# Kernel optimization log

Measured on AMD Instinct MI355X. Metric: run time of the kernel, lower is better.

## Reference

```python
import jax, jax.numpy as jnp
import numpy as np

B, S, V, D, H, DK, DFF, L = 2, 1024, 513, 512, 8, 64, 2048, 6
PAD_IDX = -1.0
EPS_GPE = 0.1

def _sinusoid_table(n_position, d_hid):
    pos = np.arange(n_position)[:, None].astype(np.float64)
    i = np.arange(d_hid)[None, :]
    angle = pos / np.power(10000.0, 2 * (i // 2) / d_hid)
    tab = np.zeros((n_position, d_hid), dtype=np.float32)
    tab[:, 0::2] = np.sin(angle[:, 0::2])
    tab[:, 1::2] = np.cos(angle[:, 1::2])
    return jnp.asarray(tab)

_POS_TABLE = _sinusoid_table(2048, D)

def _ln(x, g, b, eps=1e-6):
    m = x.mean(-1, keepdims=True)
    v = x.var(-1, keepdims=True)
    return (x - m) * jax.lax.rsqrt(v + eps) * g + b

def _mha(x_q, x_kv, wq_, wk_, wv_, wo_, mask, g, b):
    Bq, Sq, _ = x_q.shape
    Skv = x_kv.shape[1]
    q = (x_q @ wq_).reshape(Bq, Sq, H, DK).transpose(0, 2, 1, 3)
    k = (x_kv @ wk_).reshape(Bq, Skv, H, DK).transpose(0, 2, 1, 3)
    v = (x_kv @ wv_).reshape(Bq, Skv, H, DK).transpose(0, 2, 1, 3)
    scores = jnp.einsum('bhqd,bhkd->bhqk', q, k) / np.float32(np.sqrt(DK))
    scores = jnp.where(mask[:, None], scores, jnp.float32(-1e9))
    attn = jax.nn.softmax(scores, axis=-1)
    out = jnp.einsum('bhqk,bhkd->bhqd', attn, v).transpose(0, 2, 1, 3).reshape(Bq, Sq, D)
    return _ln(x_q + out @ wo_, g, b)

def _forward(dec_in, prev_dec_out, trg, adj, graph_length, gr_mask, gr_pos_enc_kernel,
             emb_w1, emb_b1, emb_w2, emb_b2, emb_w3, emb_b3, ln0_g, ln0_b,
             wq, wk, wv, wo, ln1_g, ln1_b,
             cq, ck, cv, co, ln2_g, ln2_b,
             ffn_w1, ffn_b1, ffn_w2, ffn_b2, ln3_g, ln3_b,
             p_w1, p_b1, p_w2, p_b2, p_w3, p_b3):
    # masks (n_ensemble = 1 so dec_in[:, :, 0, :] == dec_in)
    causal = jnp.tril(jnp.ones((S, S), bool))
    slf_mask = jnp.all(dec_in != PAD_IDX, -1)[:, None, :] & causal          # [B,S,S]
    enc_mask = jnp.all(prev_dec_out != PAD_IDX, -1)[:, None, :]             # [B,1,S]
    # word-embedding MLP: 513 -> 513 -> 513 -> 512
    h = jax.nn.relu(dec_in @ emb_w1 + emb_b1)
    h = jax.nn.relu(h @ emb_w2 + emb_b2)
    h = h @ emb_w3 + emb_b3                                                 # [B,S,D]
    # propagation graph positional encoding (k = 0..2, un-normalized branch)
    w = (1.0 - EPS_GPE) ** jnp.arange(gr_pos_enc_kernel.shape[1], dtype=jnp.float32)
    base = _POS_TABLE[:S]                                                   # [S,D]
    emb = jnp.einsum('k,bkst,td->bsd', w, gr_pos_enc_kernel, base) / w.sum()
    h = _ln(h + emb, ln0_g, ln0_b)
    for i in range(L):
        h = _mha(h, h, wq[i], wk[i], wv[i], wo[i], slf_mask, ln1_g[i], ln1_b[i])
        h = _mha(h, prev_dec_out, cq[i], ck[i], cv[i], co[i], enc_mask, ln2_g[i], ln2_b[i])
        f = jax.nn.relu(h @ ffn_w1[i] + ffn_b1[i]) @ ffn_w2[i] + ffn_b2[i]
        h = _ln(h + f, ln3_g[i], ln3_b[i])
    # projection head: 512 -> 513 -> 513 -> 513
    z = jax.nn.relu(h @ p_w1 + p_b1)
    z = jax.nn.relu(z @ p_w2 + p_b2)
    return z @ p_w3 + p_b3                                                  # [B,S,V]

def setup_inputs():
    key = jax.random.key(0)
    ks = jax.random.split(key, 24)
    def xavier(k, shape):
        lim = np.float32(np.sqrt(6.0 / (shape[-2] + shape[-1])))
        return jax.random.uniform(k, shape, jnp.float32, -lim, lim)
    inp = {}
    inp['dec_in'] = jax.random.uniform(ks[0], (B, S, V), jnp.float32)
    inp['prev_dec_out'] = jax.random.normal(ks[1], (B, S, D), jnp.float32)
    inp['trg'] = jnp.zeros((B, S, V), jnp.float32)
    inp['adj'] = jnp.zeros((B, S, S), jnp.float32)
    inp['graph_length'] = jnp.zeros((B, S, 10), jnp.float32)
    inp['gr_mask'] = jnp.zeros((B, 1, S, S), jnp.float32)
    gk = jax.random.uniform(ks[2], (B, 3, S, S), jnp.float32)
    inp['gr_pos_enc_kernel'] = gk / jnp.sum(gk, -1, keepdims=True)  # row-stochastic diffusion kernels
    SZ = max(V, D)  # sz_intermed = 513
    inp['emb_w1'] = xavier(ks[3], (V, SZ)); inp['emb_b1'] = jnp.zeros((SZ,))
    inp['emb_w2'] = xavier(ks[4], (SZ, SZ)); inp['emb_b2'] = jnp.zeros((SZ,))
    inp['emb_w3'] = xavier(ks[5], (SZ, D)); inp['emb_b3'] = jnp.zeros((D,))
    inp['ln0_g'] = jnp.ones((D,)); inp['ln0_b'] = jnp.zeros((D,))
    for name, ki, shp in [('wq', 6, (L, D, D)), ('wk', 7, (L, D, D)), ('wv', 8, (L, D, D)), ('wo', 9, (L, D, D)),
                          ('cq', 10, (L, D, D)), ('ck', 11, (L, D, D)), ('cv', 12, (L, D, D)), ('co', 13, (L, D, D)),
                          ('ffn_w1', 14, (L, D, DFF)), ('ffn_w2', 15, (L, DFF, D))]:
        inp[name] = xavier(ks[ki], shp)
    inp['ffn_b1'] = jnp.zeros((L, DFF)); inp['ffn_b2'] = jnp.zeros((L, D))
    inp['ln1_g'] = jnp.ones((L, D)); inp['ln1_b'] = jnp.zeros((L, D))
    inp['ln2_g'] = jnp.ones((L, D)); inp['ln2_b'] = jnp.zeros((L, D))
    inp['ln3_g'] = jnp.ones((L, D)); inp['ln3_b'] = jnp.zeros((L, D))
    inp['p_w1'] = xavier(ks[16], (D, V)); inp['p_b1'] = jnp.zeros((V,))
    inp['p_w2'] = xavier(ks[17], (V, V)); inp['p_b2'] = jnp.zeros((V,))
    inp['p_w3'] = xavier(ks[18], (V, V)); inp['p_b3'] = jnp.zeros((V,))
    return inp

def reference(dec_in, prev_dec_out, trg, adj, graph_length, gr_mask, gr_pos_enc_kernel,
              emb_w1, emb_b1, emb_w2, emb_b2, emb_w3, emb_b3, ln0_g, ln0_b,
              wq, wk, wv, wo, ln1_g, ln1_b,
              cq, ck, cv, co, ln2_g, ln2_b,
              ffn_w1, ffn_b1, ffn_w2, ffn_b2, ln3_g, ln3_b,
              p_w1, p_b1, p_w2, p_b2, p_w3, p_b3):
    return _forward(dec_in, prev_dec_out, trg, adj, graph_length, gr_mask, gr_pos_enc_kernel,
                    emb_w1, emb_b1, emb_w2, emb_b2, emb_w3, emb_b3, ln0_g, ln0_b,
                    wq, wk, wv, wo, ln1_g, ln1_b,
                    cq, ck, cv, co, ln2_g, ln2_b,
                    ffn_w1, ffn_b1, ffn_w2, ffn_b2, ln3_g, ln3_b,
                    p_w1, p_b1, p_w2, p_b2, p_w3, p_b3)
```

## Files before the change

kernel.cpp:

```cpp
#include <hip/hip_runtime.h>
#include <hip/hip_bf16.h>
#include <stdint.h>

#define BB 2
#define SS 1024
#define VV 513
#define VP 576
#define DD 512
#define HH 8
#define DKK 64
#define DFFN 2048
#define LL 6
#define MM (BB * SS)

typedef __bf16 bf16x8 __attribute__((ext_vector_type(8)));
typedef float f32x4 __attribute__((ext_vector_type(4)));
typedef unsigned short us8 __attribute__((ext_vector_type(8)));
typedef unsigned short us4 __attribute__((ext_vector_type(4)));

static __device__ inline unsigned short f2bf(float f) {
  union { float f; unsigned u; } v; v.f = f;
  unsigned u = v.u;
  unsigned r = (u + 0x7FFFu + ((u >> 16) & 1u)) >> 16;
  return (unsigned short)r;
}

static __device__ inline bf16x8 ldfrag(const unsigned short* p) {
  us8 r = *(const us8*)p;
  return __builtin_bit_cast(bf16x8, r);
}

typedef __attribute__((address_space(3))) void lds_void;
typedef const __attribute__((address_space(1))) void glb_void;
static __device__ inline void gl_lds16(const void* g, void* l) {
  __builtin_amdgcn_global_load_lds((glb_void*)g, (lds_void*)l, 16, 0, 0);
}

static __device__ inline bf16x8 ldfrag_swz(const unsigned short* base, int row, int kloc) {
  const unsigned byte = (unsigned)(row * 128 + kloc * 2) ^ (unsigned)((row & 7) << 4);
  return ldfrag((const unsigned short*)((const char*)base + byte));
}

static __device__ inline int rot3(int x) { return (x == 2) ? 0 : x + 1; }

struct GemmP {
  const unsigned short* A;
  const unsigned short* B0; const unsigned short* B1; const unsigned short* B2;
  const float* bias;
  float* C;
  unsigned short* D0; unsigned short* D1; unsigned short* D2;
  int Kp, Np, ldc, Nreal, relu;
};

template<int NB, int NT, int TRV, int KS>
__global__ __launch_bounds__(256)
void gemm_tpl(GemmP p)
{
  constexpr int FN = NT / 32;
  __shared__ unsigned short Al[3][64 * 64];
  __shared__ unsigned short Bl[3][NT * 64];
  const int tid = threadIdx.x;
  const int l = tid & 63, w = tid >> 6;
  const int wm = w >> 1, wn = w & 1;
  const int lr = l & 15, lg = l >> 4;

  const int nbn = p.Np / NT;
  int sel = 0, bx = blockIdx.x;
  if (NB > 1) { sel = bx / nbn; bx -= sel * nbn; }
  const unsigned short* Bmat = p.B0;
  if (NB > 1 && sel == 1) Bmat = p.B1;
  if (NB > 2 && sel == 2) Bmat = p.B2;
  const int m0 = blockIdx.y << 6, n0 = bx * NT;
  const int kz = (KS > 1) ? blockIdx.z : 0;

  f32x4 acc[2][FN];
  const f32x4 zf = {0.f, 0.f, 0.f, 0.f};
#pragma unroll
  for (int i = 0; i < 2; ++i)
#pragma unroll
    for (int j = 0; j < FN; ++j) acc[i][j] = zf;

  const size_t Kp = (size_t)p.Kp;
  const unsigned short* Abase = p.A + (size_t)m0 * Kp;
  const unsigned short* Bbase = Bmat + (size_t)n0 * Kp;
  const int nt = (p.Kp >> 6) / KS;
  const int kb0 = kz * nt;

  auto stage = [&](int buf, int kt) {
    const int k0 = (kb0 + kt) << 6;
#pragma unroll
    for (int j = 0; j < 2; ++j) {
      const int ti = j * 256 + tid;
      const int row = ti >> 3;
      const int ch = (ti & 7) ^ (row & 7);
      gl_lds16(Abase + (size_t)row * Kp + k0 + ch * 8, &Al[buf][ti * 8]);
    }
#pragma unroll
    for (int j = 0; j < FN; ++j) {
      const int ti = j * 256 + tid;
      const int row = ti >> 3;
      const int ch = (ti & 7) ^ (row & 7);
      gl_lds16(Bbase + (size_t)row * Kp + k0 + ch * 8, &Bl[buf][ti * 8]);
    }
  };

  stage(0, 0);
  if (nt > 1) stage(1, 1);
  int cb = 0, sb = 2;

  for (int kt = 0; kt < nt; ++kt) {
    if (kt + 1 < nt) {
      if constexpr (FN == 2) asm volatile("s_waitcnt vmcnt(4)" ::: "memory");
      else                   asm volatile("s_waitcnt vmcnt(6)" ::: "memory");
    } else {
      asm volatile("s_waitcnt vmcnt(0)" ::: "memory");
    }
    __builtin_amdgcn_s_barrier();
    if (kt + 2 < nt) { stage(sb, kt + 2); sb = rot3(sb); }
#pragma unroll
    for (int ks = 0; ks < 2; ++ks) {
      bf16x8 af[2], bfv[FN];
#pragma unroll
      for (int mf = 0; mf < 2; ++mf)
        af[mf] = ldfrag_swz(Al[cb], wm * 32 + mf * 16 + lr, ks * 32 + lg * 8);
#pragma unroll
      for (int nf = 0; nf < FN; ++nf)
        bfv[nf] = ldfrag_swz(Bl[cb], wn * (NT / 2) + nf * 16 + lr, ks * 32 + lg * 8);
#pragma unroll
      for (int mf = 0; mf < 2; ++mf)
#pragma unroll
        for (int nf = 0; nf < FN; ++nf)
          acc[mf][nf] = __builtin_amdgcn_mfma_f32_16x16x32_bf16(af[mf], bfv[nf], acc[mf][nf], 0, 0, 0);
    }
    cb = rot3(cb);
  }

  unsigned short* Dsel = p.D0;
  if (NB > 1 && sel == 1) Dsel = p.D1;
  if (NB > 2 && sel == 2) Dsel = p.D2;

  if (TRV && sel == 2) {
#pragma unroll
    for (int mf = 0; mf < 2; ++mf) {
      const int growb = m0 + wm * 32 + mf * 16 + (lg << 2);
      const int b = growb >> 10, s = growb & 1023;
#pragma unroll
      for (int nf = 0; nf < FN; ++nf) {
        const int gcol = n0 + wn * (NT / 2) + nf * 16 + lr;
        const int h = gcol >> 6, d = gcol & 63;
        us4 t;
#pragma unroll
        for (int r = 0; r < 4; ++r) t[r] = f2bf(acc[mf][nf][r]);
        *(us4*)(Dsel + (((size_t)(b * HH) + h) * DKK + d) * SS + s) = t;
      }
    }
    return;
  }

  float* Cz = p.C ? (p.C + (size_t)kz * MM * p.ldc) : nullptr;
#pragma unroll
  for (int mf = 0; mf < 2; ++mf) {
#pragma unroll
    for (int r = 0; r < 4; ++r) {
      const int grow = m0 + wm * 32 + mf * 16 + (lg << 2) + r;
#pragma unroll
      for (int nf = 0; nf < FN; ++nf) {
        const int gcol = n0 + wn * (NT / 2) + nf * 16 + lr;
        float v = acc[mf][nf][r];
        if (p.bias && kz == 0 && gcol < p.Nreal) v += p.bias[gcol];
        if (p.relu) v = fmaxf(v, 0.f);
        if (Dsel) Dsel[(size_t)grow * p.Np + gcol] = f2bf(v);
        if (Cz && gcol < p.Nreal) Cz[(size_t)grow * p.ldc + gcol] = v;
      }
    }
  }
}

struct GemmBat {
  const unsigned short* A;
  const unsigned short* B[12];
  unsigned short* D[12];
  int Kp, Np;
};

__global__ __launch_bounds__(256)
void gemm_bat(GemmBat p)
{
  __shared__ unsigned short Al[3][64 * 64];
  __shared__ unsigned short Bl[3][64 * 64];
  const int tid = threadIdx.x;
  const int l = tid & 63, w = tid >> 6;
  const int wm = w >> 1, wn = w & 1;
  const int lr = l & 15, lg = l >> 4;

  const int nbn = p.Np >> 6;
  const int sel = blockIdx.x / nbn;
  const int bx = blockIdx.x - sel * nbn;
  const unsigned short* Bmat = p.B[sel];
  unsigned short* Dmat = p.D[sel];
  const int m0 = blockIdx.y << 6, n0 = bx << 6;

  f32x4 acc[2][2];
  const f32x4 zf = {0.f, 0.f, 0.f, 0.f};
#pragma unroll
  for (int i = 0; i < 2; ++i)
#pragma unroll
    for (int j = 0; j < 2; ++j) acc[i][j] = zf;

  const size_t Kp = (size_t)p.Kp;
  const unsigned short* Abase = p.A + (size_t)m0 * Kp;
  const unsigned short* Bbase = Bmat + (size_t)n0 * Kp;

  auto stage = [&](int buf, int kt) {
    const int k0 = kt << 6;
#pragma unroll
    for (int j = 0; j < 2; ++j) {
      const int ti = j * 256 + tid;
      const int row = ti >> 3;
      const int ch = (ti & 7) ^ (row & 7);
      gl_lds16(Abase + (size_t)row * Kp + k0 + ch * 8, &Al[buf][ti * 8]);
    }
#pragma unroll
    for (int j = 0; j < 2; ++j) {
      const int ti = j * 256 + tid;
      const int row = ti >> 3;
      const int ch = (ti & 7) ^ (row & 7);
      gl_lds16(Bbase + (size_t)row * Kp + k0 + ch * 8, &Bl[buf][ti * 8]);
    }
  };

  const int nt = p.Kp >> 6;
  stage(0, 0);
  if (nt > 1) stage(1, 1);
  int cb = 0, sb = 2;

  for (int kt = 0; kt < nt; ++kt) {
    if (kt + 1 < nt) asm volatile("s_waitcnt vmcnt(4)" ::: "memory");
    else             asm volatile("s_waitcnt vmcnt(0)" ::: "memory");
    __builtin_amdgcn_s_barrier();
    if (kt + 2 < nt) { stage(sb, kt + 2); sb = rot3(sb); }
#pragma unroll
    for (int ks = 0; ks < 2; ++ks) {
      bf16x8 af[2], bfv[2];
#pragma unroll
      for (int mf = 0; mf < 2; ++mf)
        af[mf] = ldfrag_swz(Al[cb], wm * 32 + mf * 16 + lr, ks * 32 + lg * 8);
#pragma unroll
      for (int nf = 0; nf < 2; ++nf)
        bfv[nf] = ldfrag_swz(Bl[cb], wn * 32 + nf * 16 + lr, ks * 32 + lg * 8);
#pragma unroll
      for (int mf = 0; mf < 2; ++mf)
#pragma unroll
        for (int nf = 0; nf < 2; ++nf)
          acc[mf][nf] = __builtin_amdgcn_mfma_f32_16x16x32_bf16(af[mf], bfv[nf], acc[mf][nf], 0, 0, 0);
    }
    cb = rot3(cb);
  }

  if (sel & 1) {
#pragma unroll
    for (int mf = 0; mf < 2; ++mf) {
      const int growb = m0 + wm * 32 + mf * 16 + (lg << 2);
      const int b = growb >> 10, s = growb & 1023;
#pragma unroll
      for (int nf = 0; nf < 2; ++nf) {
        const int gcol = n0 + wn * 32 + nf * 16 + lr;
        const int h = gcol >> 6, d = gcol & 63;
        us4 t;
#pragma unroll
        for (int r = 0; r < 4; ++r) t[r] = f2bf(acc[mf][nf][r]);
        *(us4*)(Dmat + (((size_t)(b * HH) + h) * DKK + d) * SS + s) = t;
      }
    }
    return;
  }

#pragma unroll
  for (int mf = 0; mf < 2; ++mf) {
#pragma unroll
    for (int r = 0; r < 4; ++r) {
      const int grow = m0 + wm * 32 + mf * 16 + (lg << 2) + r;
#pragma unroll
      for (int nf = 0; nf < 2; ++nf) {
        const int gcol = n0 + wn * 32 + nf * 16 + lr;
        Dmat[(size_t)grow * p.Np + gcol] = f2bf(acc[mf][nf][r]);
      }
    }
  }
}

__global__ __launch_bounds__(128)
void attn_kernel(const unsigned short* __restrict__ Qb,
                 const unsigned short* __restrict__ Kb,
                 const unsigned short* __restrict__ VbT,
                 unsigned short* __restrict__ Ob,
                 const float* __restrict__ maskadd)
{
  __shared__ unsigned short Kl[2][2][64 * 64];
  __shared__ unsigned short Vl[2][2][64 * 64];
  __shared__ char PC[9216];
  unsigned short* Pl = (unsigned short*)PC;
  float (*comb)[66] = (float(*)[66])PC;

  const int tid = threadIdx.x;
  const int l = tid & 63, w = tid >> 6;
  const int qt = blockIdx.x, h = blockIdx.y, b = blockIdx.z;
  const int lr = l & 15, lg = l >> 4;

  bf16x8 qf[2][2];
#pragma unroll
  for (int mf = 0; mf < 2; ++mf) {
    const unsigned short* qrow = Qb + ((size_t)(b * SS) + qt * 32 + mf * 16 + lr) * DD + h * DKK;
    qf[mf][0] = ldfrag(qrow + (lg << 3));
    qf[mf][1] = ldfrag(qrow + 32 + (lg << 3));
  }

  const unsigned short* Kbase = Kb + (size_t)(b * SS) * DD + h * DKK;
  const unsigned short* Vbase = VbT + ((size_t)(b * HH) + h) * DKK * SS;

  auto stage = [&](int buf, int kt) {
#pragma unroll
    for (int j = 0; j < 8; ++j) {
      const int ti = j * 64 + l;
      const int row = ti >> 3;
      const int ch = (ti & 7) ^ (row & 7);
      gl_lds16(Kbase + (size_t)(kt * 64 + row) * DD + ch * 8, &Kl[w][buf][ti * 8]);
    }
#pragma unroll
    for (int j = 0; j < 8; ++j) {
      const int ti = j * 64 + l;
      const int row = ti >> 3;
      const int ch = (ti & 7) ^ (row & 7);
      gl_lds16(Vbase + (size_t)row * SS + kt * 64 + ch * 8, &Vl[w][buf][ti * 8]);
    }
  };

  f32x4 accO[2][4];
  const f32x4 zf = {0.f, 0.f, 0.f, 0.f};
#pragma unroll
  for (int mf = 0; mf < 2; ++mf)
#pragma unroll
    for (int nf = 0; nf < 4; ++nf) accO[mf][nf] = zf;
  float mold[2][4], lsum[2][4];
#pragma unroll
  for (int mf = 0; mf < 2; ++mf)
#pragma unroll
    for (int r = 0; r < 4; ++r) { mold[mf][r] = -1e30f; lsum[mf][r] = 0.f; }

  const int ktmax = (qt >> 1) + 1;
  const int myn = (ktmax - w + 1) >> 1;

  if (myn > 0) stage(0, w);
  int buf = 0;

  for (int i = 0; i < myn; ++i) {
    const int kt = w + 2 * i;
    if (i + 1 < myn) {
      stage(buf ^ 1, kt + 2);
      asm volatile("s_waitcnt vmcnt(16)" ::: "memory");
    } else {
      asm volatile("s_waitcnt vmcnt(0)" ::: "memory");
    }
    const unsigned short* KB = &Kl[w][buf][0];
    const unsigned short* VB = &Vl[w][buf][0];
    float sc[2][4][4];
    __builtin_amdgcn_s_setprio(1);
#pragma unroll
    for (int nf = 0; nf < 4; ++nf) {
      bf16x8 k0 = ldfrag_swz(KB, nf * 16 + lr, lg * 8);
      bf16x8 k1 = ldfrag_swz(KB, nf * 16 + lr, 32 + lg * 8);
      const int kglob = kt * 64 + nf * 16 + lr;
      const float madd = maskadd[b * SS + kglob];
#pragma unroll
      for (int mf = 0; mf < 2; ++mf) {
        f32x4 s = zf;
        s = __builtin_amdgcn_mfma_f32_16x16x32_bf16(qf[mf][0], k0, s, 0, 0, 0);
        s = __builtin_amdgcn_mfma_f32_16x16x32_bf16(qf[mf][1], k1, s, 0, 0, 0);
#pragma unroll
        for (int r = 0; r < 4; ++r) {
          const int qglob = qt * 32 + mf * 16 + (lg << 2) + r;
          sc[mf][nf][r] = (kglob > qglob) ? -1e9f : s[r] * 0.125f + madd;
        }
      }
    }
    __builtin_amdgcn_s_setprio(0);
#pragma unroll
    for (int mf = 0; mf < 2; ++mf)
#pragma unroll
      for (int r = 0; r < 4; ++r) {
        float mloc = fmaxf(fmaxf(sc[mf][0][r], sc[mf][1][r]), fmaxf(sc[mf][2][r], sc[mf][3][r]));
#pragma unroll
        for (int off = 1; off < 16; off <<= 1)
          mloc = fmaxf(mloc, __shfl_xor(mloc, off, 64));
        const float mnew = fmaxf(mold[mf][r], mloc);
        const float corr = __expf(mold[mf][r] - mnew);
        float ps = 0.f;
#pragma unroll
        for (int nf = 0; nf < 4; ++nf) {
          const float pv = __expf(sc[mf][nf][r] - mnew);
          sc[mf][nf][r] = pv;
          ps += pv;
        }
#pragma unroll
        for (int off = 1; off < 16; off <<= 1)
          ps += __shfl_xor(ps, off, 64);
        lsum[mf][r] = lsum[mf][r] * corr + ps;
#pragma unroll
        for (int nf = 0; nf < 4; ++nf) accO[mf][nf][r] *= corr;
        mold[mf][r] = mnew;
      }
    unsigned short* pw = Pl + w * 32 * 72;
#pragma unroll
    for (int mf = 0; mf < 2; ++mf)
#pragma unroll
      for (int nf = 0; nf < 4; ++nf)
#pragma unroll
        for (int r = 0; r < 4; ++r)
          pw[(mf * 16 + (lg << 2) + r) * 72 + nf * 16 + lr] = f2bf(sc[mf][nf][r]);
    bf16x8 pa[2][2];
#pragma unroll
    for (int mf = 0; mf < 2; ++mf) {
      pa[mf][0] = ldfrag(&pw[(mf * 16 + lr) * 72 + (lg << 3)]);
      pa[mf][1] = ldfrag(&pw[(mf * 16 + lr) * 72 + 32 + (lg << 3)]);
    }
    __builtin_amdgcn_s_setprio(1);
#pragma unroll
    for (int nf = 0; nf < 4; ++nf) {
      bf16x8 v0 = ldfrag_swz(VB, nf * 16 + lr, lg * 8);
      bf16x8 v1 = ldfrag_swz(VB, nf * 16 + lr, 32 + lg * 8);
#pragma unroll
      for (int mf = 0; mf < 2; ++mf) {
        accO[mf][nf] = __builtin_amdgcn_mfma_f32_16x16x32_bf16(pa[mf][0], v0, accO[mf][nf], 0, 0, 0);
        accO[mf][nf] = __builtin_amdgcn_mfma_f32_16x16x32_bf16(pa[mf][1], v1, accO[mf][nf], 0, 0, 0);
      }
    }
    __builtin_amdgcn_s_setprio(0);
    buf ^= 1;
  }

  __syncthreads();
  if (w == 1) {
#pragma unroll
    for (int mf = 0; mf < 2; ++mf)
#pragma unroll
      for (int r = 0; r < 4; ++r) {
        const int qrow = mf * 16 + (lg << 2) + r;
#pragma unroll
        for (int nf = 0; nf < 4; ++nf)
          comb[qrow][nf * 16 + lr] = accO[mf][nf][r];
        if (lr == 0) { comb[qrow][64] = mold[mf][r]; comb[qrow][65] = lsum[mf][r]; }
      }
  }
  __syncthreads();
  if (w == 0) {
#pragma unroll
    for (int mf = 0; mf < 2; ++mf)
#pragma unroll
      for (int r = 0; r < 4; ++r) {
        const int qrow = mf * 16 + (lg << 2) + r;
        const float m1 = comb[qrow][64], l1 = comb[qrow][65];
        const float m0v = mold[mf][r], l0 = lsum[mf][r];
        const float ms = fmaxf(m0v, m1);
        const float f0 = __expf(m0v - ms), f1 = __expf(m1 - ms);
        const float inv = 1.f / (l0 * f0 + l1 * f1);
        const size_t orow = ((size_t)(b * SS) + qt * 32 + mf * 16 + (lg << 2) + r) * DD + h * DKK;
#pragma unroll
        for (int nf = 0; nf < 4; ++nf)
          Ob[orow + nf * 16 + lr] =
              f2bf((accO[mf][nf][r] * f0 + comb[qrow][nf * 16 + lr] * f1) * inv);
      }
  }
}

__global__ __launch_bounds__(128)
void attnx_kernel(const unsigned short* __restrict__ Hb,
                  const unsigned short* __restrict__ Wq,
                  const unsigned short* __restrict__ Kb,
                  const unsigned short* __restrict__ VbT,
                  unsigned short* __restrict__ Ob,
                  const float* __restrict__ maskadd)
{
  __shared__ unsigned short Kl[2][2][64 * 64];
  __shared__ unsigned short Vl[2][2][64 * 64];
  __shared__ char PC[9216];
  unsigned short* Pl = (unsigned short*)PC;
  float (*comb)[66] = (float(*)[66])PC;
  unsigned short* QA = &Kl[0][0][0];
  unsigned short* QB = &Vl[0][0][0];
  unsigned short* Ql = (unsigned short*)PC;

  const int tid = threadIdx.x;
  const int l = tid & 63, w = tid >> 6;
  const int qt = blockIdx.x, h = blockIdx.y, b = blockIdx.z;
  const int lr = l & 15, lg = l >> 4;

  {
    const unsigned short* Abase = Hb + ((size_t)(b * SS) + qt * 32) * DD;
    const unsigned short* Bbase = Wq + (size_t)(h * DKK) * DD;
    auto stage_q = [&](int buf, int kt) {
      const int k0 = kt << 6;
#pragma unroll
      for (int j = 0; j < 2; ++j) {
        const int ti = j * 128 + tid;
        const int row = ti >> 3;
        const int ch = (ti & 7) ^ (row & 7);
        gl_lds16(Abase + (size_t)row * DD + k0 + ch * 8, &QA[buf * 2048 + ti * 8]);
      }
#pragma unroll
      for (int j = 0; j < 4; ++j) {
        const int ti = j * 128 + tid;
        const int row = ti >> 3;
        const int ch = (ti & 7) ^ (row & 7);
        gl_lds16(Bbase + (size_t)row * DD + k0 + ch * 8, &QB[buf * 4096 + ti * 8]);
      }
    };
    f32x4 qacc[2][2];
    const f32x4 zf = {0.f, 0.f, 0.f, 0.f};
#pragma unroll
    for (int i = 0; i < 2; ++i)
#pragma unroll
      for (int j = 0; j < 2; ++j) qacc[i][j] = zf;

    stage_q(0, 0);
    for (int kt = 0; kt < 8; ++kt) {
      if (kt + 1 < 8) {
        stage_q((kt + 1) & 1, kt + 1);
        asm volatile("s_waitcnt vmcnt(6)" ::: "memory");
      } else {
        asm volatile("s_waitcnt vmcnt(0)" ::: "memory");
      }
      __builtin_amdgcn_s_barrier();
      const unsigned short* qa = &QA[(kt & 1) * 2048];
      const unsigned short* qbuf = &QB[(kt & 1) * 4096];
#pragma unroll
      for (int ks = 0; ks < 2; ++ks) {
        bf16x8 af[2], bfv[2];
#pragma unroll
        for (int mf = 0; mf < 2; ++mf)
          af[mf] = ldfrag_swz(qa, mf * 16 + lr, ks * 32 + lg * 8);
#pragma unroll
        for (int nf = 0; nf < 2; ++nf)
          bfv[nf] = ldfrag_swz(qbuf, w * 32 + nf * 16 + lr, ks * 32 + lg * 8);
#pragma unroll
        for (int mf = 0; mf < 2; ++mf)
#pragma unroll
          for (int nf = 0; nf < 2; ++nf)
            qacc[mf][nf] = __builtin_amdgcn_mfma_f32_16x16x32_bf16(af[mf], bfv[nf], qacc[mf][nf], 0, 0, 0);
      }
      __builtin_amdgcn_s_barrier();
    }
#pragma unroll
    for (int mf = 0; mf < 2; ++mf)
#pragma unroll
      for (int nf = 0; nf < 2; ++nf)
#pragma unroll
        for (int r = 0; r < 4; ++r)
          Ql[(mf * 16 + (lg << 2) + r) * 72 + w * 32 + nf * 16 + lr] = f2bf(qacc[mf][nf][r] * 0.125f);
    __syncthreads();
  }
  bf16x8 qf[2][2];
#pragma unroll
  for (int mf = 0; mf < 2; ++mf) {
    qf[mf][0] = ldfrag(&Ql[(mf * 16 + lr) * 72 + (lg << 3)]);
    qf[mf][1] = ldfrag(&Ql[(mf * 16 + lr) * 72 + 32 + (lg << 3)]);
  }
  __syncthreads();

  const unsigned short* Kbase = Kb + (size_t)(b * SS) * DD + h * DKK;
  const unsigned short* Vbase = VbT + ((size_t)(b * HH) + h) * DKK * SS;

  auto stage = [&](int buf, int kt) {
#pragma unroll
    for (int j = 0; j < 8; ++j) {
      const int ti = j * 64 + l;
      const int row = ti >> 3;
      const int ch = (ti & 7) ^ (row & 7);
      gl_lds16(Kbase + (size_t)(kt * 64 + row) * DD + ch * 8, &Kl[w][buf][ti * 8]);
    }
#pragma unroll
    for (int j = 0; j < 8; ++j) {
      const int ti = j * 64 + l;
      const int row = ti >> 3;
      const int ch = (ti & 7) ^ (row & 7);
      gl_lds16(Vbase + (size_t)row * SS + kt * 64 + ch * 8, &Vl[w][buf][ti * 8]);
    }
  };

  f32x4 accO[2][4];
  const f32x4 zf = {0.f, 0.f, 0.f, 0.f};
#pragma unroll
  for (int mf = 0; mf < 2; ++mf)
#pragma unroll
    for (int nf = 0; nf < 4; ++nf) accO[mf][nf] = zf;
  float mold[2][4], lsum[2][4];
#pragma unroll
  for (int mf = 0; mf < 2; ++mf)
#pragma unroll
    for (int r = 0; r < 4; ++r) { mold[mf][r] = -1e30f; lsum[mf][r] = 0.f; }

  const int myn = (SS / 64 - w + 1) >> 1;
  stage(0, w);
  int buf = 0;

  for (int i = 0; i < myn; ++i) {
    const int kt = w + 2 * i;
    if (i + 1 < myn) {
      stage(buf ^ 1, kt + 2);
      asm volatile("s_waitcnt vmcnt(16)" ::: "memory");
    } else {
      asm volatile("s_waitcnt vmcnt(0)" ::: "memory");
    }
    const unsigned short* KB = &Kl[w][buf][0];
    const unsigned short* VB = &Vl[w][buf][0];
    float sc[2][4][4];
    __builtin_amdgcn_s_setprio(1);
#pragma unroll
    for (int nf = 0; nf < 4; ++nf) {
      bf16x8 k0 = ldfrag_swz(KB, nf * 16 + lr, lg * 8);
      bf16x8 k1 = ldfrag_swz(KB, nf * 16 + lr, 32 + lg * 8);
      const int kglob = kt * 64 + nf * 16 + lr;
      const float madd = maskadd[b * SS + kglob];
#pragma unroll
      for (int mf = 0; mf < 2; ++mf) {
        f32x4 s = zf;
        s = __builtin_amdgcn_mfma_f32_16x16x32_bf16(qf[mf][0], k0, s, 0, 0, 0);
        s = __builtin_amdgcn_mfma_f32_16x16x32_bf16(qf[mf][1], k1, s, 0, 0, 0);
#pragma unroll
        for (int r = 0; r < 4; ++r)
          sc[mf][nf][r] = s[r] + madd;
      }
    }
    __builtin_amdgcn_s_setprio(0);
#pragma unroll
    for (int mf = 0; mf < 2; ++mf)
#pragma unroll
      for (int r = 0; r < 4; ++r) {
        float mloc = fmaxf(fmaxf(sc[mf][0][r], sc[mf][1][r]), fmaxf(sc[mf][2][r], sc[mf][3][r]));
#pragma unroll
        for (int off = 1; off < 16; off <<= 1)
          mloc = fmaxf(mloc, __shfl_xor(mloc, off, 64));
        const float mnew = fmaxf(mold[mf][r], mloc);
        const float corr = __expf(mold[mf][r] - mnew);
        float ps = 0.f;
#pragma unroll
        for (int nf = 0; nf < 4; ++nf) {
          const float pv = __expf(sc[mf][nf][r] - mnew);
          sc[mf][nf][r] = pv;
          ps += pv;
        }
#pragma unroll
        for (int off = 1; off < 16; off <<= 1)
          ps += __shfl_xor(ps, off, 64);
        lsum[mf][r] = lsum[mf][r] * corr + ps;
#pragma unroll
        for (int nf = 0; nf < 4; ++nf) accO[mf][nf][r] *= corr;
        mold[mf][r] = mnew;
      }
    unsigned short* pw = Pl + w * 32 * 72;
#pragma unroll
    for (int mf = 0; mf < 2; ++mf)
#pragma unroll
      for (int nf = 0; nf < 4; ++nf)
#pragma unroll
        for (int r = 0; r < 4; ++r)
          pw[(mf * 16 + (lg << 2) + r) * 72 + nf * 16 + lr] = f2bf(sc[mf][nf][r]);
    bf16x8 pa[2][2];
#pragma unroll
    for (int mf = 0; mf < 2; ++mf) {
      pa[mf][0] = ldfrag(&pw[(mf * 16 + lr) * 72 + (lg << 3)]);
      pa[mf][1] = ldfrag(&pw[(mf * 16 + lr) * 72 + 32 + (lg << 3)]);
    }
    __builtin_amdgcn_s_setprio(1);
#pragma unroll
    for (int nf = 0; nf < 4; ++nf) {
      bf16x8 v0 = ldfrag_swz(VB, nf * 16 + lr, lg * 8);
      bf16x8 v1 = ldfrag_swz(VB, nf * 16 + lr, 32 + lg * 8);
#pragma unroll
      for (int mf = 0; mf < 2; ++mf) {
        accO[mf][nf] = __builtin_amdgcn_mfma_f32_16x16x32_bf16(pa[mf][0], v0, accO[mf][nf], 0, 0, 0);
        accO[mf][nf] = __builtin_amdgcn_mfma_f32_16x16x32_bf16(pa[mf][1], v1, accO[mf][nf], 0, 0, 0);
      }
    }
    __builtin_amdgcn_s_setprio(0);
    buf ^= 1;
  }

  __syncthreads();
  if (w == 1) {
#pragma unroll
    for (int mf = 0; mf < 2; ++mf)
#pragma unroll
      for (int r = 0; r < 4; ++r) {
        const int qrow = mf * 16 + (lg << 2) + r;
#pragma unroll
        for (int nf = 0; nf < 4; ++nf)
          comb[qrow][nf * 16 + lr] = accO[mf][nf][r];
        if (lr == 0) { comb[qrow][64] = mold[mf][r]; comb[qrow][65] = lsum[mf][r]; }
      }
  }
  __syncthreads();
  if (w == 0) {
#pragma unroll
    for (int mf = 0; mf < 2; ++mf)
#pragma unroll
      for (int r = 0; r < 4; ++r) {
        const int qrow = mf * 16 + (lg << 2) + r;
        const float m1 = comb[qrow][64], l1 = comb[qrow][65];
        const float m0v = mold[mf][r], l0 = lsum[mf][r];
        const float ms = fmaxf(m0v, m1);
        const float f0 = __expf(m0v - ms), f1 = __expf(m1 - ms);
        const float inv = 1.f / (l0 * f0 + l1 * f1);
        const size_t orow = ((size_t)(b * SS) + qt * 32 + mf * 16 + (lg << 2) + r) * DD + h * DKK;
#pragma unroll
        for (int nf = 0; nf < 4; ++nf)
          Ob[orow + nf * 16 + lr] =
              f2bf((accO[mf][nf][r] * f0 + comb[qrow][nf * 16 + lr] * f1) * inv);
      }
  }
}

template<int P>
__global__ __launch_bounds__(256)
void addln_kernel(const float* __restrict__ a, const float* __restrict__ c,
                  const float* __restrict__ g, const float* __restrict__ bb,
                  float* __restrict__ hf, unsigned short* __restrict__ hb)
{
  const int row = blockIdx.x * 4 + (threadIdx.x >> 6);
  const int l = threadIdx.x & 63;
  const float* ar = a + (size_t)row * DD + l * 8;
  f32x4 x0 = *(const f32x4*)ar;
  f32x4 x1 = *(const f32x4*)(ar + 4);
#pragma unroll
  for (int pp = 0; pp < P; ++pp) {
    const float* cr = c + (size_t)pp * MM * DD + (size_t)row * DD + l * 8;
    x0 += *(const f32x4*)cr;
    x1 += *(const f32x4*)(cr + 4);
  }
  float sum = x0[0] + x0[1] + x0[2] + x0[3] + x1[0] + x1[1] + x1[2] + x1[3];
#pragma unroll
  for (int off = 1; off < 64; off <<= 1) sum += __shfl_xor(sum, off, 64);
  const float mean = sum * (1.f / 512.f);
  float vs = 0.f;
#pragma unroll
  for (int j = 0; j < 4; ++j) { float d0 = x0[j] - mean; float d1 = x1[j] - mean; vs += d0 * d0 + d1 * d1; }
#pragma unroll
  for (int off = 1; off < 64; off <<= 1) vs += __shfl_xor(vs, off, 64);
  const float rs = rsqrtf(vs * (1.f / 512.f) + 1e-6f);
  const f32x4 g0 = *(const f32x4*)(g + l * 8), g1 = *(const f32x4*)(g + l * 8 + 4);
  const f32x4 b0 = *(const f32x4*)(bb + l * 8), b1 = *(const f32x4*)(bb + l * 8 + 4);
  f32x4 o0, o1;
  us8 ob;
#pragma unroll
  for (int j = 0; j < 4; ++j) {
    o0[j] = (x0[j] - mean) * rs * g0[j] + b0[j];
    o1[j] = (x1[j] - mean) * rs * g1[j] + b1[j];
    ob[j] = f2bf(o0[j]); ob[j + 4] = f2bf(o1[j]);
  }
  float* of = hf + (size_t)row * DD + l * 8;
  *(f32x4*)of = o0; *(f32x4*)(of + 4) = o1;
  *(us8*)(hb + (size_t)row * DD + l * 8) = ob;
}

__global__ __launch_bounds__(256)
void prep_all(const float* __restrict__ dec_in, const float* __restrict__ prev,
              unsigned short* __restrict__ decb, unsigned short* __restrict__ prevb,
              float* __restrict__ kvs, float* __restrict__ kve,
              unsigned short* __restrict__ tabT,
              const float* __restrict__ gk, unsigned short* __restrict__ Mb)
{
  const int blk = blockIdx.x, tid = threadIdx.x;
  if (blk < 1024) {
    const int isdec = blk < 512;
    const int row = (isdec ? blk : blk - 512) * 4 + (tid >> 6);
    const int l = tid & 63;
    const int NC = isdec ? VV : DD, NP = isdec ? VP : DD;
    const float* xr = (isdec ? dec_in : prev) + (size_t)row * NC;
    unsigned short* ob = (isdec ? decb : prevb) + (size_t)row * NP;
    int ok = 1;
    for (int j = l; j < NP; j += 64) {
      if (j < NC) {
        const float v = xr[j];
        ok &= (v != -1.0f) ? 1 : 0;
        ob[j] = f2bf(v);
      } else ob[j] = 0;
    }
    ok = __all(ok) ? 1 : 0;
    if (l == 0) (isdec ? kvs : kve)[row] = ok ? 0.f : -1e9f;
  } else if (blk < 3072) {
    const int i = (blk - 1024) * 256 + tid;
    const int d = i >> 10, s = i & 1023;
    const float ex = (float)(2 * (d >> 1)) * (1.0f / (float)DD);
    const float ang = (float)s * exp2f(ex * -13.287712379549449f);
    tabT[i] = f2bf((d & 1) ? cosf(ang) : sinf(ang));
  } else {
    const int i = (blk - 3072) * 256 + tid;
    const int b = i / (SS * SS);
    const int rem = i - b * (SS * SS);
    const float* p = gk + (size_t)b * 3 * SS * SS + rem;
    Mb[i] = f2bf((p[0] + 0.9f * p[SS * SS] + 0.81f * p[2 * SS * SS]) * (1.0f / 2.71f));
  }
}

struct WJobs {
  const float* W[8]; unsigned short* WT[8];
  int K[8], N[8], Kp[8], Np[8], nbx[8], nby[8];
  int off[9];
};
__global__ __launch_bounds__(256)
void wconv_all(WJobs p)
{
  __shared__ float t[64][65];
  const int bid = blockIdx.x;
  int j = 0;
#pragma unroll
  for (int i = 0; i < 8; ++i) if (bid >= p.off[i + 1]) j = i + 1;
  const int local = bid - p.off[j];
  const int per = p.nbx[j] * p.nby[j];
  const int z = local / per;
  const int rem = local - z * per;
  const int by = rem / p.nbx[j];
  const int bx = rem - by * p.nbx[j];
  const int K = p.K[j], N = p.N[j], Kp = p.Kp[j], Np = p.Np[j];
  const float* Wl = p.W[j] + (size_t)z * K * N;
  unsigned short* WTl = p.WT[j] + (size_t)z * Np * Kp;
  const int n0 = bx << 6, k0 = by << 6;
  const int cx = threadIdx.x & 63, ry = threadIdx.x >> 6;
#pragma unroll
  for (int i = 0; i < 16; ++i) {
    const int kk = k0 + ry + i * 4, nn = n0 + cx;
    t[ry + i * 4][cx] = (kk < K && nn < N) ? Wl[(size_t)kk * N + nn] : 0.f;
  }
  __syncthreads();
#pragma unroll
  for (int i = 0; i < 16; ++i) {
    const int nn = n0 + ry + i * 4, kk = k0 + cx;
    if (nn < Np && kk < Kp) WTl[(size_t)nn * Kp + kk] = f2bf(t[cx][ry + i * 4]);
  }
}

struct WconvB { const float* W[8]; unsigned short* WT[8]; };
__global__ __launch_bounds__(256)
void wconv8_kernel(WconvB p)
{
  __shared__ float t[64][65];
  const int z = blockIdx.z;
  const int wi = z / LL, li = z - wi * LL;
  const float* Wl = p.W[wi] + (size_t)li * DD * DD;
  unsigned short* WTl = p.WT[wi] + (size_t)li * DD * DD;
  const int n0 = blockIdx.x << 6, k0 = blockIdx.y << 6;
  const int cx = threadIdx.x & 63, ry = threadIdx.x >> 6;
#pragma unroll
  for (int i = 0; i < 16; ++i)
    t[ry + i * 4][cx] = Wl[(size_t)(k0 + ry + i * 4) * DD + n0 + cx];
  __syncthreads();
#pragma unroll
  for (int i = 0; i < 16; ++i)
    WTl[(size_t)(n0 + ry + i * 4) * DD + k0 + cx] = f2bf(t[cx][ry + i * 4]);
}

static inline void g1(hipStream_t s, const unsigned short* A, const unsigned short* B,
                      const float* bias, float* C, unsigned short* D,
                      int Kp, int Np, int ldc, int Nreal, int relu)
{
  GemmP p{};
  p.A = A; p.B0 = B; p.bias = bias; p.C = C; p.D0 = D;
  p.Kp = Kp; p.Np = Np; p.ldc = ldc; p.Nreal = Nreal; p.relu = relu;
  gemm_tpl<1, 64, 0, 1><<<dim3(Np >> 6, MM >> 6), 256, 0, s>>>(p);
}

static inline void g1w(hipStream_t s, const unsigned short* A, const unsigned short* B,
                       const float* bias, unsigned short* D, int Kp, int Np, int relu)
{
  GemmP p{};
  p.A = A; p.B0 = B; p.bias = bias; p.D0 = D;
  p.Kp = Kp; p.Np = Np; p.ldc = Np; p.Nreal = Np; p.relu = relu;
  gemm_tpl<1, 128, 0, 1><<<dim3(Np >> 7, MM >> 6), 256, 0, s>>>(p);
}

template<int KS>
static inline void g1k(hipStream_t s, const unsigned short* A, const unsigned short* B,
                       const float* bias, float* C, int Kp)
{
  GemmP p{};
  p.A = A; p.B0 = B; p.bias = bias; p.C = C;
  p.Kp = Kp; p.Np = DD; p.ldc = DD; p.Nreal = DD; p.relu = 0;
  gemm_tpl<1, 64, 0, KS><<<dim3(DD >> 6, MM >> 6, KS), 256, 0, s>>>(p);
}

static inline void g3t(hipStream_t s, const unsigned short* A, const unsigned short* B0,
                       const unsigned short* B1, const unsigned short* B2,
                       unsigned short* D0, unsigned short* D1, unsigned short* D2T)
{
  GemmP p{};
  p.A = A; p.B0 = B0; p.B1 = B1; p.B2 = B2; p.D0 = D0; p.D1 = D1; p.D2 = D2T;
  p.Kp = DD; p.Np = DD; p.ldc = DD; p.Nreal = DD; p.relu = 0;
  gemm_tpl<3, 64, 1, 1><<<dim3(3 * (DD >> 6), MM >> 6), 256, 0, s>>>(p);
}

extern "C" void kernel_launch(void* const* d_in, const int* in_sizes, int n_in,
                              void* d_out, int out_size, void* d_ws, size_t ws_size,
                              hipStream_t stream)
{
  (void)in_sizes; (void)n_in; (void)out_size; (void)ws_size;
  const float* dec_in = (const float*)d_in[0];
  const float* prev   = (const float*)d_in[1];
  const float* gk     = (const float*)d_in[6];
  const float* emb_w1 = (const float*)d_in[7];
  const float* emb_b1 = (const float*)d_in[8];
  const float* emb_w2 = (const float*)d_in[9];
  const float* emb_b2 = (const float*)d_in[10];
  const float* emb_w3 = (const float*)d_in[11];
  const float* emb_b3 = (const float*)d_in[12];
  const float* ln0_g  = (const float*)d_in[13];
  const float* ln0_b  = (const float*)d_in[14];
  const float* wq     = (const float*)d_in[15];
  const float* wk     = (const float*)d_in[16];
  const float* wv     = (const float*)d_in[17];
  const float* wo     = (const float*)d_in[18];
  const float* cq     = (const float*)d_in[19];
  const float* ck     = (const float*)d_in[20];
  const float* cv     = (const float*)d_in[21];
  const float* co     = (const float*)d_in[22];
  const float* ffn_w1 = (const float*)d_in[23];
  const float* ffn_w2 = (const float*)d_in[24];
  const float* ffn_b1 = (const float*)d_in[25];
  const float* ffn_b2 = (const float*)d_in[26];
  const float* ln1_g  = (const float*)d_in[27];
  const float* ln1_b  = (const float*)d_in[28];
  const float* ln2_g  = (const float*)d_in[29];
  const float* ln2_b  = (const float*)d_in[30];
  const float* ln3_g  = (const float*)d_in[31];
  const float* ln3_b  = (const float*)d_in[32];
  const float* p_w1   = (const float*)d_in[33];
  const float* p_b1   = (const float*)d_in[34];
  const float* p_w2   = (const float*)d_in[35];
  const float* p_b2   = (const float*)d_in[36];
  const float* p_w3   = (const float*)d_in[37];
  const float* p_b3   = (const float*)d_in[38];

  char* wsp = (char*)d_ws;
  auto carve = [&](size_t bytes) { char* r = wsp; wsp += (bytes + 255) & ~(size_t)255; return r; };

  unsigned short* decb  = (unsigned short*)carve((size_t)MM * VP * 2);
  unsigned short* prevb = (unsigned short*)carve((size_t)MM * DD * 2);
  float*          hf    = (float*)carve((size_t)MM * DD * 4);
  unsigned short* hb    = (unsigned short*)carve((size_t)MM * DD * 2);
  float*          xf1   = (float*)carve((size_t)MM * DD * 4);
  unsigned short* tb1   = (unsigned short*)carve((size_t)MM * DFFN * 2);
  unsigned short* Mbb   = tb1;
  float*          xf2   = (float*)((char*)tb1 + (size_t)MM * SS * 2);
  unsigned short* tb2a  = (unsigned short*)carve((size_t)MM * VP * 2);
  unsigned short* tb2b  = (unsigned short*)carve((size_t)MM * VP * 2);
  unsigned short* qb    = (unsigned short*)carve((size_t)MM * DD * 2);
  unsigned short* kb    = (unsigned short*)carve((size_t)MM * DD * 2);
  unsigned short* vbT   = (unsigned short*)carve((size_t)MM * DD * 2);
  float* kvs = (float*)carve((size_t)MM * 4);
  float* kve = (float*)carve((size_t)MM * 4);
  unsigned short* postabt = (unsigned short*)carve((size_t)DD * SS * 2);
  unsigned short* ew1t  = (unsigned short*)carve((size_t)VP * VP * 2);
  unsigned short* ew2t  = (unsigned short*)carve((size_t)VP * VP * 2);
  unsigned short* ew3t  = (unsigned short*)carve((size_t)DD * VP * 2);
  unsigned short* wqt   = (unsigned short*)carve((size_t)LL * DD * DD * 2);
  unsigned short* wkt   = (unsigned short*)carve((size_t)LL * DD * DD * 2);
  unsigned short* wvt   = (unsigned short*)carve((size_t)LL * DD * DD * 2);
  unsigned short* wot   = (unsigned short*)carve((size_t)LL * DD * DD * 2);
  unsigned short* cqt   = (unsigned short*)carve((size_t)LL * DD * DD * 2);
  unsigned short* ckt   = (unsigned short*)carve((size_t)LL * DD * DD * 2);
  unsigned short* cvt   = (unsigned short*)carve((size_t)LL * DD * DD * 2);
  unsigned short* cot   = (unsigned short*)carve((size_t)LL * DD * DD * 2);
  unsigned short* f1t   = (unsigned short*)carve((size_t)LL * DFFN * DD * 2);
  unsigned short* f2t   = (unsigned short*)carve((size_t)LL * DD * DFFN * 2);
  unsigned short* p1t   = (unsigned short*)carve((size_t)VP * DD * 2);
  unsigned short* p2t   = (unsigned short*)carve((size_t)VP * VP * 2);
  unsigned short* p3t   = (unsigned short*)carve((size_t)VP * VP * 2);
  unsigned short* ckall = (unsigned short*)carve((size_t)LL * MM * DD * 2);
  unsigned short* cvbT  = (unsigned short*)carve((size_t)LL * MM * DD * 2);
  float*          xk4   = (float*)carve((size_t)4 * MM * DD * 4);

  const dim3 agrid(SS / 32, HH, BB);

  prep_all<<<11264, 256, 0, stream>>>(dec_in, prev, decb, prevb, kvs, kve, postabt, gk, Mbb);

  {
    WconvB wb{};
    wb.W[0] = wq; wb.W[1] = wk; wb.W[2] = wv; wb.W[3] = wo;
    wb.W[4] = cq; wb.W[5] = ck; wb.W[6] = cv; wb.W[7] = co;
    wb.WT[0] = wqt; wb.WT[1] = wkt; wb.WT[2] = wvt; wb.WT[3] = wot;
    wb.WT[4] = cqt; wb.WT[5] = ckt; wb.WT[6] = cvt; wb.WT[7] = cot;
    wconv8_kernel<<<dim3(8, 8, 8 * LL), 256, 0, stream>>>(wb);
  }
  {
    WJobs wj{};
    const float* Ws[8]   = {emb_w1, emb_w2, emb_w3, ffn_w1, ffn_w2, p_w1, p_w2, p_w3};
    unsigned short* Ds[8] = {ew1t, ew2t, ew3t, f1t, f2t, p1t, p2t, p3t};
    const int Ks[8]  = {VV, VV, VV, DD, DFFN, DD, VV, VV};
    const int Ns[8]  = {VV, VV, DD, DFFN, DD, VV, VV, VV};
    const int Kps[8] = {VP, VP, VP, DD, DFFN, DD, VP, VP};
    const int Nps[8] = {VP, VP, DD, DFFN, DD, VP, VP, VP};
    const int nls[8] = {1, 1, 1, LL, LL, 1, 1, 1};
    int off = 0;
    for (int j = 0; j < 8; ++j) {
      wj.W[j] = Ws[j]; wj.WT[j] = Ds[j];
      wj.K[j] = Ks[j]; wj.N[j] = Ns[j]; wj.Kp[j] = Kps[j]; wj.Np[j] = Nps[j];
      wj.nbx[j] = (Nps[j] + 63) / 64; wj.nby[j] = (Kps[j] + 63) / 64;
      wj.off[j] = off;
      off += wj.nbx[j] * wj.nby[j] * nls[j];
    }
    wj.off[8] = off;
    wconv_all<<<off, 256, 0, stream>>>(wj);
  }

  {
    GemmBat p{};
    p.A = prevb; p.Kp = DD; p.Np = DD;
    for (int i = 0; i < LL; ++i) {
      p.B[2 * i]     = ckt + (size_t)i * DD * DD;
      p.B[2 * i + 1] = cvt + (size_t)i * DD * DD;
      p.D[2 * i]     = ckall + (size_t)i * MM * DD;
      p.D[2 * i + 1] = cvbT + (size_t)i * MM * DD;
    }
    gemm_bat<<<dim3(12 * (DD >> 6), MM >> 6), 256, 0, stream>>>(p);
  }

  g1(stream, decb, ew1t, emb_b1, nullptr, tb2a, VP, VP, VP, VV, 1);
  g1(stream, tb2a, ew2t, emb_b2, nullptr, tb2b, VP, VP, VP, VV, 1);
  g1(stream, tb2b, ew3t, emb_b3, xf1, nullptr, VP, DD, DD, DD, 0);
  g1(stream, Mbb, postabt, nullptr, xf2, nullptr, SS, DD, DD, DD, 0);
  addln_kernel<1><<<MM / 4, 256, 0, stream>>>(xf1, xf2, ln0_g, ln0_b, hf, hb);

  for (int i = 0; i < LL; ++i) {
    const size_t od = (size_t)i * DD * DD;
    g3t(stream, hb, wqt + od, wkt + od, wvt + od, qb, kb, vbT);
    attn_kernel<<<agrid, 128, 0, stream>>>(qb, kb, vbT, qb, kvs);
    g1k<2>(stream, qb, wot + od, nullptr, xk4, DD);
    addln_kernel<2><<<MM / 4, 256, 0, stream>>>(hf, xk4, ln1_g + i * DD, ln1_b + i * DD, hf, hb);
    attnx_kernel<<<agrid, 128, 0, stream>>>(hb, cqt + od, ckall + (size_t)i * MM * DD,
                                            cvbT + (size_t)i * MM * DD, qb, kve);
    g1k<2>(stream, qb, cot + od, nullptr, xk4, DD);
    addln_kernel<2><<<MM / 4, 256, 0, stream>>>(hf, xk4, ln2_g + i * DD, ln2_b + i * DD, hf, hb);
    g1w(stream, hb, f1t + (size_t)i * DFFN * DD, ffn_b1 + i * DFFN, tb1, DD, DFFN, 1);
    g1k<4>(stream, tb1, f2t + (size_t)i * DD * DFFN, ffn_b2 + i * DD, xk4, DFFN);
    addln_kernel<4><<<MM / 4, 256, 0, stream>>>(hf, xk4, ln3_g + i * DD, ln3_b + i * DD, hf, hb);
  }

  g1(stream, hb, p1t, p_b1, nullptr, tb2a, DD, VP, VP, VV, 1);
  g1(stream, tb2a, p2t, p_b2, nullptr, tb2b, VP, VP, VP, VV, 1);
  g1(stream, tb2b, p3t, p_b3, (float*)d_out, nullptr, VP, VP, VV, VV, 0);
}
```

Before: 994.0 us.

## Fuse FFN GEMMs and layernorm into one cooperative kernel; merge prologue launches

Replaces the per-layer FFN sequence (up-projection GEMM, split-K down-projection GEMM, add+layernorm) with a single cooperative kernel that runs persistent work loops separated by grid-wide syncs. It also merges the three prologue kernels (input prep and the two weight-conversion kernels) into one launch and switches the positional-encoding GEMM to split-K. The aim is to cut kernel launch overhead and tail gaps between dependent stages. The cost is grid.sync overhead, and the grid is capped at 512 blocks, which may leave parallelism unused in the GEMM phases.

```diff
diff --git a/kernel.cpp b/kernel.cpp
--- a/kernel.cpp
+++ b/kernel.cpp
@@ -1,6 +1,9 @@
 #include <hip/hip_runtime.h>
 #include <hip/hip_bf16.h>
+#include <hip/hip_cooperative_groups.h>
 #include <stdint.h>
+
+namespace cg = cooperative_groups;
 
 #define BB 2
 #define SS 1024
@@ -43,6 +46,171 @@
 
 static __device__ inline int rot3(int x) { return (x == 2) ? 0 : x + 1; }
 
+template<int NT>
+__device__ __forceinline__ void gemm_item(
+    unsigned short* Al, unsigned short* Bl,
+    const unsigned short* Abase, const unsigned short* Bbase,
+    int Kp, int nt, int kb0,
+    const float* bias, int applybias, int relu,
+    unsigned short* D, int ldD, int m0, int n0,
+    float* Cz, int ldc)
+{
+  constexpr int FN = NT / 32;
+  const int tid = threadIdx.x;
+  const int l = tid & 63, w = tid >> 6;
+  const int wm = w >> 1, wn = w & 1;
+  const int lr = l & 15, lg = l >> 4;
+
+  f32x4 acc[2][FN];
+  const f32x4 zf = {0.f, 0.f, 0.f, 0.f};
+#pragma unroll
+  for (int i = 0; i < 2; ++i)
+#pragma unroll
+    for (int j = 0; j < FN; ++j) acc[i][j] = zf;
+
+  auto stage = [&](int buf, int kt) {
+    const int k0 = (kb0 + kt) << 6;
+#pragma unroll
+    for (int j = 0; j < 2; ++j) {
+      const int ti = j * 256 + tid;
+      const int row = ti >> 3;
+      const int ch = (ti & 7) ^ (row & 7);
+      gl_lds16(Abase + (size_t)row * Kp + k0 + ch * 8, &Al[buf * 4096 + ti * 8]);
+    }
+#pragma unroll
+    for (int j = 0; j < FN; ++j) {
+      const int ti = j * 256 + tid;
+      const int row = ti >> 3;
+      const int ch = (ti & 7) ^ (row & 7);
+      gl_lds16(Bbase + (size_t)row * Kp + k0 + ch * 8, &Bl[buf * (NT * 64) + ti * 8]);
+    }
+  };
+
+  stage(0, 0);
+  if (nt > 1) stage(1, 1);
+  int cb = 0, sb = 2;
+
+  for (int kt = 0; kt < nt; ++kt) {
+    if (kt + 1 < nt) {
+      if constexpr (FN == 2) asm volatile("s_waitcnt vmcnt(4)" ::: "memory");
+      else                   asm volatile("s_waitcnt vmcnt(6)" ::: "memory");
+    } else {
+      asm volatile("s_waitcnt vmcnt(0)" ::: "memory");
+    }
+    __builtin_amdgcn_s_barrier();
+    if (kt + 2 < nt) { stage(sb, kt + 2); sb = rot3(sb); }
+#pragma unroll
+    for (int ks = 0; ks < 2; ++ks) {
+      bf16x8 af[2], bfv[FN];
+#pragma unroll
+      for (int mf = 0; mf < 2; ++mf)
+        af[mf] = ldfrag_swz(Al + cb * 4096, wm * 32 + mf * 16 + lr, ks * 32 + lg * 8);
+#pragma unroll
+      for (int nf = 0; nf < FN; ++nf)
+        bfv[nf] = ldfrag_swz(Bl + cb * (NT * 64), wn * (NT / 2) + nf * 16 + lr, ks * 32 + lg * 8);
+#pragma unroll
+      for (int mf = 0; mf < 2; ++mf)
+#pragma unroll
+        for (int nf = 0; nf < FN; ++nf)
+          acc[mf][nf] = __builtin_amdgcn_mfma_f32_16x16x32_bf16(af[mf], bfv[nf], acc[mf][nf], 0, 0, 0);
+    }
+    cb = rot3(cb);
+  }
+
+#pragma unroll
+  for (int mf = 0; mf < 2; ++mf) {
+#pragma unroll
+    for (int r = 0; r < 4; ++r) {
+      const int grow = m0 + wm * 32 + mf * 16 + (lg << 2) + r;
+#pragma unroll
+      for (int nf = 0; nf < FN; ++nf) {
+        const int gcol = n0 + wn * (NT / 2) + nf * 16 + lr;
+        float v = acc[mf][nf][r];
+        if (bias && applybias) v += bias[gcol];
+        if (relu) v = fmaxf(v, 0.f);
+        if (D) D[(size_t)grow * ldD + gcol] = f2bf(v);
+        if (Cz) Cz[(size_t)grow * ldc + gcol] = v;
+      }
+    }
+  }
+}
+
+template<int P>
+__device__ __forceinline__ void addln_item(int wi, const float* a, const float* c,
+    const float* g, const float* bb, float* hf, unsigned short* hb)
+{
+  const int row = wi * 4 + (threadIdx.x >> 6);
+  const int l = threadIdx.x & 63;
+  const float* ar = a + (size_t)row * DD + l * 8;
+  f32x4 x0 = *(const f32x4*)ar;
+  f32x4 x1 = *(const f32x4*)(ar + 4);
+#pragma unroll
+  for (int pp = 0; pp < P; ++pp) {
+    const float* cr = c + (size_t)pp * MM * DD + (size_t)row * DD + l * 8;
+    x0 += *(const f32x4*)cr;
+    x1 += *(const f32x4*)(cr + 4);
+  }
+  float sum = x0[0] + x0[1] + x0[2] + x0[3] + x1[0] + x1[1] + x1[2] + x1[3];
+#pragma unroll
+  for (int off = 1; off < 64; off <<= 1) sum += __shfl_xor(sum, off, 64);
+  const float mean = sum * (1.f / 512.f);
+  float vs = 0.f;
+#pragma unroll
+  for (int j = 0; j < 4; ++j) { float d0 = x0[j] - mean; float d1 = x1[j] - mean; vs += d0 * d0 + d1 * d1; }
+#pragma unroll
+  for (int off = 1; off < 64; off <<= 1) vs += __shfl_xor(vs, off, 64);
+  const float rs = rsqrtf(vs * (1.f / 512.f) + 1e-6f);
+  const f32x4 g0 = *(const f32x4*)(g + l * 8), g1 = *(const f32x4*)(g + l * 8 + 4);
+  const f32x4 b0 = *(const f32x4*)(bb + l * 8), b1 = *(const f32x4*)(bb + l * 8 + 4);
+  f32x4 o0, o1;
+  us8 ob;
+#pragma unroll
+  for (int j = 0; j < 4; ++j) {
+    o0[j] = (x0[j] - mean) * rs * g0[j] + b0[j];
+    o1[j] = (x1[j] - mean) * rs * g1[j] + b1[j];
+    ob[j] = f2bf(o0[j]); ob[j + 4] = f2bf(o1[j]);
+  }
+  float* of = hf + (size_t)row * DD + l * 8;
+  *(f32x4*)of = o0; *(f32x4*)(of + 4) = o1;
+  *(us8*)(hb + (size_t)row * DD + l * 8) = ob;
+}
+
+struct FfnP {
+  const unsigned short* hb;
+  const unsigned short* f1t; const float* b1;
+  unsigned short* tb1;
+  const unsigned short* f2t; const float* b2;
+  float* xk4;
+  const float* hf; const float* gamma; const float* beta;
+  float* hfout; unsigned short* hbout;
+};
+
+__global__ __launch_bounds__(256)
+void coop_ffn(FfnP p)
+{
+  __shared__ unsigned short Al[3 * 4096];
+  __shared__ unsigned short Bl[3 * 128 * 64];
+  cg::grid_group grid = cg::this_grid();
+
+  for (int wi = blockIdx.x; wi < 512; wi += gridDim.x) {
+    const int bx = wi & 15, by = wi >> 4;
+    gemm_item<128>(Al, Bl,
+                   p.hb + (size_t)(by * 64) * DD, p.f1t + (size_t)(bx * 128) * DD,
+                   DD, 8, 0, p.b1, 1, 1, p.tb1, DFFN, by * 64, bx * 128, nullptr, 0);
+  }
+  grid.sync();
+  for (int wi = blockIdx.x; wi < 1024; wi += gridDim.x) {
+    const int kz = wi >> 8, rem = wi & 255, by = rem >> 3, bx = rem & 7;
+    gemm_item<64>(Al, Bl,
+                  p.tb1 + (size_t)(by * 64) * DFFN, p.f2t + (size_t)(bx * 64) * DFFN,
+                  DFFN, 8, kz * 8, p.b2, kz == 0, 0, nullptr, 0, by * 64, bx * 64,
+                  p.xk4 + (size_t)kz * MM * DD, DD);
+  }
+  grid.sync();
+  for (int wi = blockIdx.x; wi < 512; wi += gridDim.x)
+    addln_item<4>(wi, p.hf, p.xk4, p.gamma, p.beta, p.hfout, p.hbout);
+}
+
 struct GemmP {
   const unsigned short* A;
   const unsigned short* B0; const unsigned short* B1; const unsigned short* B2;
@@ -57,8 +225,8 @@
 void gemm_tpl(GemmP p)
 {
   constexpr int FN = NT / 32;
-  __shared__ unsigned short Al[3][64 * 64];
-  __shared__ unsigned short Bl[3][NT * 64];
+  __shared__ unsigned short Al[3 * 4096];
+  __shared__ unsigned short Bl[3 * NT * 64];
   const int tid = threadIdx.x;
   const int l = tid & 63, w = tid >> 6;
   const int wm = w >> 1, wn = w & 1;
@@ -73,6 +241,16 @@
   const int m0 = blockIdx.y << 6, n0 = bx * NT;
   const int kz = (KS > 1) ? blockIdx.z : 0;
 
+  if (!(TRV && sel == 2)) {
+    unsigned short* Dsel = p.D0;
+    if (NB > 1 && sel == 1) Dsel = p.D1;
+    float* Cz = p.C ? (p.C + (size_t)kz * MM * p.ldc) : nullptr;
+    gemm_item<NT>(Al, Bl, p.A + (size_t)m0 * p.Kp, Bmat + (size_t)n0 * p.Kp,
+                  p.Kp, (p.Kp >> 6) / KS, kz * ((p.Kp >> 6) / KS),
+                  p.bias, kz == 0, p.relu, Dsel, p.Np, m0, n0, Cz, p.ldc);
+    return;
+  }
+
   f32x4 acc[2][FN];
   const f32x4 zf = {0.f, 0.f, 0.f, 0.f};
 #pragma unroll
@@ -83,38 +261,32 @@
   const size_t Kp = (size_t)p.Kp;
   const unsigned short* Abase = p.A + (size_t)m0 * Kp;
   const unsigned short* Bbase = Bmat + (size_t)n0 * Kp;
-  const int nt = (p.Kp >> 6) / KS;
-  const int kb0 = kz * nt;
+  const int nt = p.Kp >> 6;
 
   auto stage = [&](int buf, int kt) {
-    const int k0 = (kb0 + kt) << 6;
+    const int k0 = kt << 6;
 #pragma unroll
     for (int j = 0; j < 2; ++j) {
       const int ti = j * 256 + tid;
       const int row = ti >> 3;
       const int ch = (ti & 7) ^ (row & 7);
-      gl_lds16(Abase + (size_t)row * Kp + k0 + ch * 8, &Al[buf][ti * 8]);
+      gl_lds16(Abase + (size_t)row * Kp + k0 + ch * 8, &Al[buf * 4096 + ti * 8]);
     }
 #pragma unroll
     for (int j = 0; j < FN; ++j) {
       const int ti = j * 256 + tid;
       const int row = ti >> 3;
       const int ch = (ti & 7) ^ (row & 7);
-      gl_lds16(Bbase + (size_t)row * Kp + k0 + ch * 8, &Bl[buf][ti * 8]);
+      gl_lds16(Bbase + (size_t)row * Kp + k0 + ch * 8, &Bl[buf * (NT * 64) + ti * 8]);
     }
   };
 
   stage(0, 0);
   if (nt > 1) stage(1, 1);
   int cb = 0, sb = 2;
-
   for (int kt = 0; kt < nt; ++kt) {
-    if (kt + 1 < nt) {
-      if constexpr (FN == 2) asm volatile("s_waitcnt vmcnt(4)" ::: "memory");
-      else                   asm volatile("s_waitcnt vmcnt(6)" ::: "memory");
-    } else {
-      asm volatile("s_waitcnt vmcnt(0)" ::: "memory");
-    }
+    if (kt + 1 < nt) asm volatile("s_waitcnt vmcnt(4)" ::: "memory");
+    else             asm volatile("s_waitcnt vmcnt(0)" ::: "memory");
     __builtin_amdgcn_s_barrier();
     if (kt + 2 < nt) { stage(sb, kt + 2); sb = rot3(sb); }
 #pragma unroll
@@ -122,10 +294,10 @@
       bf16x8 af[2], bfv[FN];
 #pragma unroll
       for (int mf = 0; mf < 2; ++mf)
-        af[mf] = ldfrag_swz(Al[cb], wm * 32 + mf * 16 + lr, ks * 32 + lg * 8);
+        af[mf] = ldfrag_swz(Al + cb * 4096, wm * 32 + mf * 16 + lr, ks * 32 + lg * 8);
 #pragma unroll
       for (int nf = 0; nf < FN; ++nf)
-        bfv[nf] = ldfrag_swz(Bl[cb], wn * (NT / 2) + nf * 16 + lr, ks * 32 + lg * 8);
+        bfv[nf] = ldfrag_swz(Bl + cb * (NT * 64), wn * (NT / 2) + nf * 16 + lr, ks * 32 + lg * 8);
 #pragma unroll
       for (int mf = 0; mf < 2; ++mf)
 #pragma unroll
@@ -134,43 +306,100 @@
     }
     cb = rot3(cb);
   }
-
-  unsigned short* Dsel = p.D0;
-  if (NB > 1 && sel == 1) Dsel = p.D1;
-  if (NB > 2 && sel == 2) Dsel = p.D2;
-
-  if (TRV && sel == 2) {
-#pragma unroll
-    for (int mf = 0; mf < 2; ++mf) {
-      const int growb = m0 + wm * 32 + mf * 16 + (lg << 2);
-      const int b = growb >> 10, s = growb & 1023;
-#pragma unroll
-      for (int nf = 0; nf < FN; ++nf) {
-        const int gcol = n0 + wn * (NT / 2) + nf * 16 + lr;
-        const int h = gcol >> 6, d = gcol & 63;
-        us4 t;
-#pragma unroll
-        for (int r = 0; r < 4; ++r) t[r] = f2bf(acc[mf][nf][r]);
-        *(us4*)(Dsel + (((size_t)(b * HH) + h) * DKK + d) * SS + s) = t;
-      }
-    }
-    return;
-  }
-
-  float* Cz = p.C ? (p.C + (size_t)kz * MM * p.ldc) : nullptr;
+#pragma unroll
+  for (int mf = 0; mf < 2; ++mf) {
+    const int growb = m0 + wm * 32 + mf * 16 + (lg << 2);
+    const int b = growb >> 10, s = growb & 1023;
+#pragma unroll
+    for (int nf = 0; nf < FN; ++nf) {
+      const int gcol = n0 + wn * (NT / 2) + nf * 16 + lr;
+      const int h = gcol >> 6, d = gcol & 63;
+      us4 t;
+#pragma unroll
+      for (int r = 0; r < 4; ++r) t[r] = f2bf(acc[mf][nf][r]);
+      *(us4*)(p.D2 + (((size_t)(b * HH) + h) * DKK + d) * SS + s) = t;
+    }
+  }
+}
+
+__global__ __launch_bounds__(256)
+void gemm_f32(GemmP p)
+{
+  __shared__ unsigned short Al[3 * 4096];
+  __shared__ unsigned short Bl[3 * 4096];
+  const int tid = threadIdx.x;
+  const int l = tid & 63, w = tid >> 6;
+  const int wm = w >> 1, wn = w & 1;
+  const int lr = l & 15, lg = l >> 4;
+  const int m0 = blockIdx.y << 6, n0 = blockIdx.x << 6;
+
+  f32x4 acc[2][2];
+  const f32x4 zf = {0.f, 0.f, 0.f, 0.f};
+#pragma unroll
+  for (int i = 0; i < 2; ++i)
+#pragma unroll
+    for (int j = 0; j < 2; ++j) acc[i][j] = zf;
+
+  const size_t Kp = (size_t)p.Kp;
+  const unsigned short* Abase = p.A + (size_t)m0 * Kp;
+  const unsigned short* Bbase = p.B0 + (size_t)n0 * Kp;
+  const int nt = p.Kp >> 6;
+
+  auto stage = [&](int buf, int kt) {
+    const int k0 = kt << 6;
+#pragma unroll
+    for (int j = 0; j < 2; ++j) {
+      const int ti = j * 256 + tid;
+      const int row = ti >> 3;
+      const int ch = (ti & 7) ^ (row & 7);
+      gl_lds16(Abase + (size_t)row * Kp + k0 + ch * 8, &Al[buf * 4096 + ti * 8]);
+    }
+#pragma unroll
+    for (int j = 0; j < 2; ++j) {
+      const int ti = j * 256 + tid;
+      const int row = ti >> 3;
+      const int ch = (ti & 7) ^ (row & 7);
+      gl_lds16(Bbase + (size_t)row * Kp + k0 + ch * 8, &Bl[buf * 4096 + ti * 8]);
+    }
+  };
+  stage(0, 0);
+  if (nt > 1) stage(1, 1);
+  int cb = 0, sb = 2;
+  for (int kt = 0; kt < nt; ++kt) {
+    if (kt + 1 < nt) asm volatile("s_waitcnt vmcnt(4)" ::: "memory");
+    else             asm volatile("s_waitcnt vmcnt(0)" ::: "memory");
+    __builtin_amdgcn_s_barrier();
+    if (kt + 2 < nt) { stage(sb, kt + 2); sb = rot3(sb); }
+#pragma unroll
+    for (int ks = 0; ks < 2; ++ks) {
+      bf16x8 af[2], bfv[2];
+#pragma unroll
+      for (int mf = 0; mf < 2; ++mf)
+        af[mf] = ldfrag_swz(Al + cb * 4096, wm * 32 + mf * 16 + lr, ks * 32 + lg * 8);
+#pragma unroll
+      for (int nf = 0; nf < 2; ++nf)
+        bfv[nf] = ldfrag_swz(Bl + cb * 4096, wn * 32 + nf * 16 + lr, ks * 32 + lg * 8);
+#pragma unroll
+      for (int mf = 0; mf < 2; ++mf)
+#pragma unroll
+        for (int nf = 0; nf < 2; ++nf)
+          acc[mf][nf] = __builtin_amdgcn_mfma_f32_16x16x32_bf16(af[mf], bfv[nf], acc[mf][nf], 0, 0, 0);
+    }
+    cb = rot3(cb);
+  }
 #pragma unroll
   for (int mf = 0; mf < 2; ++mf) {
 #pragma unroll
     for (int r = 0; r < 4; ++r) {
       const int grow = m0 + wm * 32 + mf * 16 + (lg << 2) + r;
 #pragma unroll
-      for (int nf = 0; nf < FN; ++nf) {
-        const int gcol = n0 + wn * (NT / 2) + nf * 16 + lr;
+      for (int nf = 0; nf < 2; ++nf) {
+        const int gcol = n0 + wn * 32 + nf * 16 + lr;
         float v = acc[mf][nf][r];
-        if (p.bias && kz == 0 && gcol < p.Nreal) v += p.bias[gcol];
+        if (p.bias && gcol < p.Nreal) v += p.bias[gcol];
         if (p.relu) v = fmaxf(v, 0.f);
-        if (Dsel) Dsel[(size_t)grow * p.Np + gcol] = f2bf(v);
-        if (Cz && gcol < p.Nreal) Cz[(size_t)grow * p.ldc + gcol] = v;
+        if (p.D0) p.D0[(size_t)grow * p.Np + gcol] = f2bf(v);
+        if (p.C && gcol < p.Nreal) p.C[(size_t)grow * p.ldc + gcol] = v;
       }
     }
   }
@@ -186,8 +415,8 @@
 __global__ __launch_bounds__(256)
 void gemm_bat(GemmBat p)
 {
-  __shared__ unsigned short Al[3][64 * 64];
-  __shared__ unsigned short Bl[3][64 * 64];
+  __shared__ unsigned short Al[3 * 4096];
+  __shared__ unsigned short Bl[3 * 4096];
   const int tid = threadIdx.x;
   const int l = tid & 63, w = tid >> 6;
   const int wm = w >> 1, wn = w & 1;
@@ -218,14 +447,14 @@
       const int ti = j * 256 + tid;
       const int row = ti >> 3;
       const int ch = (ti & 7) ^ (row & 7);
-      gl_lds16(Abase + (size_t)row * Kp + k0 + ch * 8, &Al[buf][ti * 8]);
+      gl_lds16(Abase + (size_t)row * Kp + k0 + ch * 8, &Al[buf * 4096 + ti * 8]);
     }
 #pragma unroll
     for (int j = 0; j < 2; ++j) {
       const int ti = j * 256 + tid;
       const int row = ti >> 3;
       const int ch = (ti & 7) ^ (row & 7);
-      gl_lds16(Bbase + (size_t)row * Kp + k0 + ch * 8, &Bl[buf][ti * 8]);
+      gl_lds16(Bbase + (size_t)row * Kp + k0 + ch * 8, &Bl[buf * 4096 + ti * 8]);
     }
   };
 
@@ -244,10 +473,10 @@
       bf16x8 af[2], bfv[2];
 #pragma unroll
       for (int mf = 0; mf < 2; ++mf)
-        af[mf] = ldfrag_swz(Al[cb], wm * 32 + mf * 16 + lr, ks * 32 + lg * 8);
+        af[mf] = ldfrag_swz(Al + cb * 4096, wm * 32 + mf * 16 + lr, ks * 32 + lg * 8);
 #pragma unroll
       for (int nf = 0; nf < 2; ++nf)
-        bfv[nf] = ldfrag_swz(Bl[cb], wn * 32 + nf * 16 + lr, ks * 32 + lg * 8);
+        bfv[nf] = ldfrag_swz(Bl + cb * 4096, wn * 32 + nf * 16 + lr, ks * 32 + lg * 8);
 #pragma unroll
       for (int mf = 0; mf < 2; ++mf)
 #pragma unroll
@@ -725,57 +954,31 @@
                   const float* __restrict__ g, const float* __restrict__ bb,
                   float* __restrict__ hf, unsigned short* __restrict__ hb)
 {
-  const int row = blockIdx.x * 4 + (threadIdx.x >> 6);
-  const int l = threadIdx.x & 63;
-  const float* ar = a + (size_t)row * DD + l * 8;
-  f32x4 x0 = *(const f32x4*)ar;
-  f32x4 x1 = *(const f32x4*)(ar + 4);
-#pragma unroll
-  for (int pp = 0; pp < P; ++pp) {
-    const float* cr = c + (size_t)pp * MM * DD + (size_t)row * DD + l * 8;
-    x0 += *(const f32x4*)cr;
-    x1 += *(const f32x4*)(cr + 4);
-  }
-  float sum = x0[0] + x0[1] + x0[2] + x0[3] + x1[0] + x1[1] + x1[2] + x1[3];
-#pragma unroll
-  for (int off = 1; off < 64; off <<= 1) sum += __shfl_xor(sum, off, 64);
-  const float mean = sum * (1.f / 512.f);
-  float vs = 0.f;
-#pragma unroll
-  for (int j = 0; j < 4; ++j) { float d0 = x0[j] - mean; float d1 = x1[j] - mean; vs += d0 * d0 + d1 * d1; }
-#pragma unroll
-  for (int off = 1; off < 64; off <<= 1) vs += __shfl_xor(vs, off, 64);
-  const float rs = rsqrtf(vs * (1.f / 512.f) + 1e-6f);
-  const f32x4 g0 = *(const f32x4*)(g + l * 8), g1 = *(const f32x4*)(g + l * 8 + 4);
-  const f32x4 b0 = *(const f32x4*)(bb + l * 8), b1 = *(const f32x4*)(bb + l * 8 + 4);
-  f32x4 o0, o1;
-  us8 ob;
-#pragma unroll
-  for (int j = 0; j < 4; ++j) {
-    o0[j] = (x0[j] - mean) * rs * g0[j] + b0[j];
-    o1[j] = (x1[j] - mean) * rs * g1[j] + b1[j];
-    ob[j] = f2bf(o0[j]); ob[j + 4] = f2bf(o1[j]);
-  }
-  float* of = hf + (size_t)row * DD + l * 8;
-  *(f32x4*)of = o0; *(f32x4*)(of + 4) = o1;
-  *(us8*)(hb + (size_t)row * DD + l * 8) = ob;
-}
+  addln_item<P>(blockIdx.x, a, c, g, bb, hf, hb);
+}
+
+struct ProP {
+  const float *dec_in, *prev, *gk;
+  unsigned short *decb, *prevb, *tabT, *Mb;
+  float *kvs, *kve;
+  const float* W8[8]; unsigned short* WT8[8];
+  const float* W[8]; unsigned short* WT[8];
+  int K[8], N[8], Kp[8], Np[8], nbx[8], nby[8];
+  int off[9];
+};
 
 __global__ __launch_bounds__(256)
-void prep_all(const float* __restrict__ dec_in, const float* __restrict__ prev,
-              unsigned short* __restrict__ decb, unsigned short* __restrict__ prevb,
-              float* __restrict__ kvs, float* __restrict__ kve,
-              unsigned short* __restrict__ tabT,
-              const float* __restrict__ gk, unsigned short* __restrict__ Mb)
-{
-  const int blk = blockIdx.x, tid = threadIdx.x;
-  if (blk < 1024) {
-    const int isdec = blk < 512;
-    const int row = (isdec ? blk : blk - 512) * 4 + (tid >> 6);
+void prologue_all(ProP p)
+{
+  __shared__ float t[64][65];
+  const int bid = blockIdx.x, tid = threadIdx.x;
+  if (bid < 1024) {
+    const int isdec = bid < 512;
+    const int row = (isdec ? bid : bid - 512) * 4 + (tid >> 6);
     const int l = tid & 63;
     const int NC = isdec ? VV : DD, NP = isdec ? VP : DD;
-    const float* xr = (isdec ? dec_in : prev) + (size_t)row * NC;
-    unsigned short* ob = (isdec ? decb : prevb) + (size_t)row * NP;
+    const float* xr = (isdec ? p.dec_in : p.prev) + (size_t)row * NC;
+    unsigned short* ob = (isdec ? p.decb : p.prevb) + (size_t)row * NP;
     int ok = 1;
     for (int j = l; j < NP; j += 64) {
       if (j < NC) {
@@ -785,77 +988,64 @@
       } else ob[j] = 0;
     }
     ok = __all(ok) ? 1 : 0;
-    if (l == 0) (isdec ? kvs : kve)[row] = ok ? 0.f : -1e9f;
-  } else if (blk < 3072) {
-    const int i = (blk - 1024) * 256 + tid;
+    if (l == 0) (isdec ? p.kvs : p.kve)[row] = ok ? 0.f : -1e9f;
+  } else if (bid < 3072) {
+    const int i = (bid - 1024) * 256 + tid;
     const int d = i >> 10, s = i & 1023;
     const float ex = (float)(2 * (d >> 1)) * (1.0f / (float)DD);
     const float ang = (float)s * exp2f(ex * -13.287712379549449f);
-    tabT[i] = f2bf((d & 1) ? cosf(ang) : sinf(ang));
-  } else {
-    const int i = (blk - 3072) * 256 + tid;
+    p.tabT[i] = f2bf((d & 1) ? cosf(ang) : sinf(ang));
+  } else if (bid < 11264) {
+    const int i = (bid - 3072) * 256 + tid;
     const int b = i / (SS * SS);
     const int rem = i - b * (SS * SS);
-    const float* p = gk + (size_t)b * 3 * SS * SS + rem;
-    Mb[i] = f2bf((p[0] + 0.9f * p[SS * SS] + 0.81f * p[2 * SS * SS]) * (1.0f / 2.71f));
-  }
-}
-
-struct WJobs {
-  const float* W[8]; unsigned short* WT[8];
-  int K[8], N[8], Kp[8], Np[8], nbx[8], nby[8];
-  int off[9];
-};
-__global__ __launch_bounds__(256)
-void wconv_all(WJobs p)
-{
-  __shared__ float t[64][65];
-  const int bid = blockIdx.x;
-  int j = 0;
-#pragma unroll
-  for (int i = 0; i < 8; ++i) if (bid >= p.off[i + 1]) j = i + 1;
-  const int local = bid - p.off[j];
-  const int per = p.nbx[j] * p.nby[j];
-  const int z = local / per;
-  const int rem = local - z * per;
-  const int by = rem / p.nbx[j];
-  const int bx = rem - by * p.nbx[j];
-  const int K = p.K[j], N = p.N[j], Kp = p.Kp[j], Np = p.Np[j];
-  const float* Wl = p.W[j] + (size_t)z * K * N;
-  unsigned short* WTl = p.WT[j] + (size_t)z * Np * Kp;
-  const int n0 = bx << 6, k0 = by << 6;
-  const int cx = threadIdx.x & 63, ry = threadIdx.x >> 6;
-#pragma unroll
-  for (int i = 0; i < 16; ++i) {
-    const int kk = k0 + ry + i * 4, nn = n0 + cx;
-    t[ry + i * 4][cx] = (kk < K && nn < N) ? Wl[(size_t)kk * N + nn] : 0.f;
-  }
-  __syncthreads();
-#pragma unroll
-  for (int i = 0; i < 16; ++i) {
-    const int nn = n0 + ry + i * 4, kk = k0 + cx;
-    if (nn < Np && kk < Kp) WTl[(size_t)nn * Kp + kk] = f2bf(t[cx][ry + i * 4]);
-  }
-}
-
-struct WconvB { const float* W[8]; unsigned short* WT[8]; };
-__global__ __launch_bounds__(256)
-void wconv8_kernel(WconvB p)
-{
-  __shared__ float t[64][65];
-  const int z = blockIdx.z;
-  const int wi = z / LL, li = z - wi * LL;
-  const float* Wl = p.W[wi] + (size_t)li * DD * DD;
-  unsigned short* WTl = p.WT[wi] + (size_t)li * DD * DD;
-  const int n0 = blockIdx.x << 6, k0 = blockIdx.y << 6;
-  const int cx = threadIdx.x & 63, ry = threadIdx.x >> 6;
-#pragma unroll
-  for (int i = 0; i < 16; ++i)
-    t[ry + i * 4][cx] = Wl[(size_t)(k0 + ry + i * 4) * DD + n0 + cx];
-  __syncthreads();
-#pragma unroll
-  for (int i = 0; i < 16; ++i)
-    WTl[(size_t)(n0 + ry + i * 4) * DD + k0 + cx] = f2bf(t[cx][ry + i * 4]);
+    const float* q = p.gk + (size_t)b * 3 * SS * SS + rem;
+    p.Mb[i] = f2bf((q[0] + 0.9f * q[SS * SS] + 0.81f * q[2 * SS * SS]) * (1.0f / 2.71f));
+  } else if (bid < 11264 + 3072) {
+    const int idx = bid - 11264;
+    const int z = idx >> 6;
+    const int rem = idx & 63;
+    const int by = rem >> 3, bx = rem & 7;
+    const int wi = z / LL, li = z - wi * LL;
+    const float* Wl = p.W8[wi] + (size_t)li * DD * DD;
+    unsigned short* WTl = p.WT8[wi] + (size_t)li * DD * DD;
+    const int n0 = bx << 6, k0 = by << 6;
+    const int cx = tid & 63, ry = tid >> 6;
+#pragma unroll
+    for (int i = 0; i < 16; ++i)
+      t[ry + i * 4][cx] = Wl[(size_t)(k0 + ry + i * 4) * DD + n0 + cx];
+    __syncthreads();
+#pragma unroll
+    for (int i = 0; i < 16; ++i)
+      WTl[(size_t)(n0 + ry + i * 4) * DD + k0 + cx] = f2bf(t[cx][ry + i * 4]);
+  } else {
+    const int bid2 = bid - 11264 - 3072;
+    int j = 0;
+#pragma unroll
+    for (int i = 0; i < 8; ++i) if (bid2 >= p.off[i + 1]) j = i + 1;
+    const int local = bid2 - p.off[j];
+    const int per = p.nbx[j] * p.nby[j];
+    const int z = local / per;
+    const int rem = local - z * per;
+    const int by = rem / p.nbx[j];
+    const int bx = rem - by * p.nbx[j];
+    const int K = p.K[j], N = p.N[j], Kp = p.Kp[j], Np = p.Np[j];
+    const float* Wl = p.W[j] + (size_t)z * K * N;
+    unsigned short* WTl = p.WT[j] + (size_t)z * Np * Kp;
+    const int n0 = bx << 6, k0 = by << 6;
+    const int cx = tid & 63, ry = tid >> 6;
+#pragma unroll
+    for (int i = 0; i < 16; ++i) {
+      const int kk = k0 + ry + i * 4, nn = n0 + cx;
+      t[ry + i * 4][cx] = (kk < K && nn < N) ? Wl[(size_t)kk * N + nn] : 0.f;
+    }
+    __syncthreads();
+#pragma unroll
+    for (int i = 0; i < 16; ++i) {
+      const int nn = n0 + ry + i * 4, kk = k0 + cx;
+      if (nn < Np && kk < Kp) WTl[(size_t)nn * Kp + kk] = f2bf(t[cx][ry + i * 4]);
+    }
+  }
 }
 
 static inline void g1(hipStream_t s, const unsigned short* A, const unsigned short* B,
@@ -865,16 +1055,7 @@
   GemmP p{};
   p.A = A; p.B0 = B; p.bias = bias; p.C = C; p.D0 = D;
   p.Kp = Kp; p.Np = Np; p.ldc = ldc; p.Nreal = Nreal; p.relu = relu;
-  gemm_tpl<1, 64, 0, 1><<<dim3(Np >> 6, MM >> 6), 256, 0, s>>>(p);
-}
-
-static inline void g1w(hipStream_t s, const unsigned short* A, const unsigned short* B,
-                       const float* bias, unsigned short* D, int Kp, int Np, int relu)
-{
-  GemmP p{};
-  p.A = A; p.B0 = B; p.bias = bias; p.D0 = D;
-  p.Kp = Kp; p.Np = Np; p.ldc = Np; p.Nreal = Np; p.relu = relu;
-  gemm_tpl<1, 128, 0, 1><<<dim3(Np >> 7, MM >> 6), 256, 0, s>>>(p);
+  gemm_f32<<<dim3(Np >> 6, MM >> 6), 256, 0, s>>>(p);
 }
 
 template<int KS>
@@ -948,7 +1129,6 @@
   float*          xf1   = (float*)carve((size_t)MM * DD * 4);
   unsigned short* tb1   = (unsigned short*)carve((size_t)MM * DFFN * 2);
   unsigned short* Mbb   = tb1;
-  float*          xf2   = (float*)((char*)tb1 + (size_t)MM * SS * 2);
   unsigned short* tb2a  = (unsigned short*)carve((size_t)MM * VP * 2);
   unsigned short* tb2b  = (unsigned short*)carve((size_t)MM * VP * 2);
   unsigned short* qb    = (unsigned short*)carve((size_t)MM * DD * 2);
@@ -979,19 +1159,15 @@
 
   const dim3 agrid(SS / 32, HH, BB);
 
-  prep_all<<<11264, 256, 0, stream>>>(dec_in, prev, decb, prevb, kvs, kve, postabt, gk, Mbb);
-
   {
-    WconvB wb{};
-    wb.W[0] = wq; wb.W[1] = wk; wb.W[2] = wv; wb.W[3] = wo;
-    wb.W[4] = cq; wb.W[5] = ck; wb.W[6] = cv; wb.W[7] = co;
-    wb.WT[0] = wqt; wb.WT[1] = wkt; wb.WT[2] = wvt; wb.WT[3] = wot;
-    wb.WT[4] = cqt; wb.WT[5] = ckt; wb.WT[6] = cvt; wb.WT[7] = cot;
-    wconv8_kernel<<<dim3(8, 8, 8 * LL), 256, 0, stream>>>(wb);
-  }
-  {
-    WJobs wj{};
-    const float* Ws[8]   = {emb_w1, emb_w2, emb_w3, ffn_w1, ffn_w2, p_w1, p_w2, p_w3};
+    ProP pp{};
+    pp.dec_in = dec_in; pp.prev = prev; pp.gk = gk;
+    pp.decb = decb; pp.prevb = prevb; pp.tabT = postabt; pp.Mb = Mbb;
+    pp.kvs = kvs; pp.kve = kve;
+    const float* W8s[8] = {wq, wk, wv, wo, cq, ck, cv, co};
+    unsigned short* WT8s[8] = {wqt, wkt, wvt, wot, cqt, ckt, cvt, cot};
+    for (int i = 0; i < 8; ++i) { pp.W8[i] = W8s[i]; pp.WT8[i] = WT8s[i]; }
+    const float* Ws[8]    = {emb_w1, emb_w2, emb_w3, ffn_w1, ffn_w2, p_w1, p_w2, p_w3};
     unsigned short* Ds[8] = {ew1t, ew2t, ew3t, f1t, f2t, p1t, p2t, p3t};
     const int Ks[8]  = {VV, VV, VV, DD, DFFN, DD, VV, VV};
     const int Ns[8]  = {VV, VV, DD, DFFN, DD, VV, VV, VV};
@@ -1000,14 +1176,14 @@
     const int nls[8] = {1, 1, 1, LL, LL, 1, 1, 1};
     int off = 0;
     for (int j = 0; j < 8; ++j) {
-      wj.W[j] = Ws[j]; wj.WT[j] = Ds[j];
-      wj.K[j] = Ks[j]; wj.N[j] = Ns[j]; wj.Kp[j] = Kps[j]; wj.Np[j] = Nps[j];
-      wj.nbx[j] = (Nps[j] + 63) / 64; wj.nby[j] = (Kps[j] + 63) / 64;
-      wj.off[j] = off;
-      off += wj.nbx[j] * wj.nby[j] * nls[j];
-    }
-    wj.off[8] = off;
-    wconv_all<<<off, 256, 0, stream>>>(wj);
+      pp.W[j] = Ws[j]; pp.WT[j] = Ds[j];
+      pp.K[j] = Ks[j]; pp.N[j] = Ns[j]; pp.Kp[j] = Kps[j]; pp.Np[j] = Nps[j];
+      pp.nbx[j] = (Nps[j] + 63) / 64; pp.nby[j] = (Kps[j] + 63) / 64;
+      pp.off[j] = off;
+      off += pp.nbx[j] * pp.nby[j] * nls[j];
+    }
+    pp.off[8] = off;
+    prologue_all<<<11264 + 3072 + off, 256, 0, stream>>>(pp);
   }
 
   {
@@ -1025,8 +1201,14 @@
   g1(stream, decb, ew1t, emb_b1, nullptr, tb2a, VP, VP, VP, VV, 1);
   g1(stream, tb2a, ew2t, emb_b2, nullptr, tb2b, VP, VP, VP, VV, 1);
   g1(stream, tb2b, ew3t, emb_b3, xf1, nullptr, VP, DD, DD, DD, 0);
-  g1(stream, Mbb, postabt, nullptr, xf2, nullptr, SS, DD, DD, DD, 0);
-  addln_kernel<1><<<MM / 4, 256, 0, stream>>>(xf1, xf2, ln0_g, ln0_b, hf, hb);
+  g1k<4>(stream, Mbb, postabt, nullptr, xk4, SS);
+  addln_kernel<4><<<MM / 4, 256, 0, stream>>>(xf1, xk4, ln0_g, ln0_b, hf, hb);
+
+  int coopBlocks = 2;
+  hipOccupancyMaxActiveBlocksPerMultiprocessor(&coopBlocks, (const void*)coop_ffn, 256, 0);
+  if (coopBlocks < 1) coopBlocks = 1;
+  int coopGrid = coopBlocks * 256;
+  if (coopGrid > 512) coopGrid = 512;
 
   for (int i = 0; i < LL; ++i) {
     const size_t od = (size_t)i * DD * DD;
@@ -1038,9 +1220,19 @@
                                             cvbT + (size_t)i * MM * DD, qb, kve);
     g1k<2>(stream, qb, cot + od, nullptr, xk4, DD);
     addln_kernel<2><<<MM / 4, 256, 0, stream>>>(hf, xk4, ln2_g + i * DD, ln2_b + i * DD, hf, hb);
-    g1w(stream, hb, f1t + (size_t)i * DFFN * DD, ffn_b1 + i * DFFN, tb1, DD, DFFN, 1);
-    g1k<4>(stream, tb1, f2t + (size_t)i * DD * DFFN, ffn_b2 + i * DD, xk4, DFFN);
-    addln_kernel<4><<<MM / 4, 256, 0, stream>>>(hf, xk4, ln3_g + i * DD, ln3_b + i * DD, hf, hb);
+    {
+      FfnP fp{};
+      fp.hb = hb;
+      fp.f1t = f1t + (size_t)i * DFFN * DD; fp.b1 = ffn_b1 + i * DFFN;
+      fp.tb1 = tb1;
+      fp.f2t = f2t + (size_t)i * DD * DFFN; fp.b2 = ffn_b2 + i * DD;
+      fp.xk4 = xk4;
+      fp.hf = hf; fp.gamma = ln3_g + i * DD; fp.beta = ln3_b + i * DD;
+      fp.hfout = hf; fp.hbout = hb;
+      void* kargs[] = {&fp};
+      hipLaunchCooperativeKernel((const void*)coop_ffn, dim3(coopGrid), dim3(256),
+                                 kargs, 0, stream);
+    }
   }
 
   g1(stream, hb, p1t, p_b1, nullptr, tb2a, DD, VP, VP, VV, 1);
```

Result: slower. 1.499 ms (+50.8%).
